# Kernel tuning notes

Hardware: AMD Instinct MI355X
Metric: run time of the kernel (lower is better)

Reference implementation:

```python
import jax, jax.numpy as jnp
import numpy as np

N, E, F_IN, H, C, Q = 4096, 131072, 512, 64, 16, 6
ALPHA = 1.0
NITER = 2  # torch.svd_lowrank default power iterations


def setup_inputs() -> dict:
    key = jax.random.key(0)
    ks = jax.random.split(key, 12)
    rn = lambda k, s, sc=0.05: jax.random.normal(k, s, dtype=jnp.float32) * sc
    return {
        'x': jax.random.normal(ks[0], (N, F_IN), dtype=jnp.float32),
        'edge_index': jax.random.randint(ks[1], (2, E), 0, N, dtype=jnp.int32),
        'gcn1_w': rn(ks[2], (F_IN, H)), 'gcn1_b': jnp.zeros((H,), jnp.float32),
        'gcn2_w': rn(ks[3], (H, C)), 'gcn2_b': jnp.zeros((C,), jnp.float32),
        'ptd1_w1': rn(ks[4], (F_IN, H)), 'ptd1_b1': jnp.zeros((H,), jnp.float32),
        'ptd1_w2': rn(ks[5], (H, 1)), 'ptd1_b2': jnp.zeros((1,), jnp.float32),
        'ptd2_w1': rn(ks[6], (H, 32)), 'ptd2_b1': jnp.zeros((32,), jnp.float32),
        'ptd2_w2': rn(ks[7], (32, 1)), 'ptd2_b2': jnp.zeros((1,), jnp.float32),
        'omega1': jax.random.normal(ks[8], (N, Q), dtype=jnp.float32),
        'omega2': jax.random.normal(ks[9], (N, Q), dtype=jnp.float32),
    }


def _mlp2(x, w1, b1, w2, b2):
    return jax.nn.relu(x @ w1 + b1) @ w2 + b2


def _edge_gate(x, src, dst, w1, b1, w2, b2):
    # agg = ptd(x_src - x_dst)**2 ; test branch: s = alpha*sigmoid(agg), clipped to [0,1]
    agg = _mlp2(x[src] - x[dst], w1, b1, w2, b2)
    agg = agg * agg
    s = ALPHA * jax.nn.sigmoid(agg)
    return jnp.clip(s.reshape(-1), 0.0, 1.0)


def _gcn_conv(x, src, dst, ew, w, b):
    # PyG GCNConv with edge_weight: add self-loops (weight 1), symmetric norm, aggregate src->dst
    h = x @ w
    si = jnp.arange(N)
    s_full = jnp.concatenate([src, si])
    d_full = jnp.concatenate([dst, si])
    ew_full = jnp.concatenate([ew, jnp.ones((N,), ew.dtype)])
    deg = jax.ops.segment_sum(ew_full, d_full, num_segments=N)
    dis = jnp.where(deg > 0, jax.lax.rsqrt(jnp.maximum(deg, 1e-12)), 0.0)
    norm = dis[s_full] * ew_full * dis[d_full]
    out = jax.ops.segment_sum(norm[:, None] * h[s_full], d_full, num_segments=N)
    return out + b


def _svd_lowrank_V(A, omega):
    # torch.svd_lowrank(A, q=6, niter=2): randomized range finder + small SVD; returns V [N, Q]
    Qb, _ = jnp.linalg.qr(A @ omega)
    for _ in range(NITER):
        Z, _ = jnp.linalg.qr(A.T @ Qb)
        Qb, _ = jnp.linalg.qr(A @ Z)
    B = Qb.T @ A  # [Q, N]
    _, _, Vh = jnp.linalg.svd(B, full_matrices=False)
    return Vh.T  # [N, Q]


def _nuc_loss(aa, V, deflate_matmul):
    loss = jnp.float32(0.0)
    for k in range(Q):  # fixed small Q=6, structurally sequential deflation
        vi = aa @ V[:, k:k + 1]  # [N,1]
        vi = vi / jnp.linalg.norm(vi)
        vmv = (vi.T @ (aa @ vi))[0, 0]
        vv = (vi.T @ vi)[0, 0]
        loss = loss + jnp.sqrt(jnp.abs(vmv / vv))
        if k > 1:
            outer = vi @ vi.T
            aa = aa - (aa @ outer if deflate_matmul else aa * outer)
    return loss


def reference(x, edge_index, gcn1_w, gcn1_b, gcn2_w, gcn2_b,
              ptd1_w1, ptd1_b1, ptd1_w2, ptd1_b2,
              ptd2_w1, ptd2_b1, ptd2_w2, ptd2_b2, omega1, omega2):
    src, dst = edge_index[0], edge_index[1]

    s_1 = _edge_gate(x, src, dst, ptd1_w1, ptd1_b1, ptd1_w2, ptd1_b2)  # [E]
    x1 = jax.nn.relu(_gcn_conv(x, src, dst, s_1, gcn1_w, gcn1_b))  # [N,H], dropout off (eval)

    s_2 = _edge_gate(x1, src, dst, ptd2_w1, ptd2_b1, ptd2_w2, ptd2_b2)  # [E]
    x_out = _gcn_conv(x1, src, dst, s_2, gcn2_w, gcn2_b)  # [N,C]

    # consistency loss: MSE of centered gates against zeros
    consist = jnp.mean((s_1 - jnp.mean(s_1)) ** 2) + jnp.mean((s_2 - jnp.mean(s_2)) ** 2)

    # dense adjacencies (duplicate edges sum, as in to_dense_adj)
    s1d = jnp.zeros((N, N), jnp.float32).at[src, dst].add(s_1) + 1e-6
    s2d = jnp.zeros((N, N), jnp.float32).at[src, dst].add(s_2) + 1e-6
    aa1 = s1d @ s1d.T
    aa2 = s2d @ s2d.T

    V1 = _svd_lowrank_V(s1d, omega1)
    V2 = _svd_lowrank_V(s2d, omega2)
    nuc = _nuc_loss(aa1, V1, deflate_matmul=False) + _nuc_loss(aa2, V2, deflate_matmul=True)

    top2 = jax.lax.top_k(x_out, 2)[0]
    calib = -top2[:, 0] + top2[:, 1]

    return (jax.nn.log_softmax(x_out, axis=1),
            jax.nn.softmax(x_out, axis=1),
            0.01 * consist + 0.01 * nuc,
            s_1, s_2, jnp.mean(calib))
```

## Files before the change

### kernel.cpp

```cpp
#include <hip/hip_runtime.h>
#include <cmath>

constexpr int N = 4096;
constexpr int EDG = 131072;
constexpr float GEPS = 1e-6f;

__device__ __forceinline__ float* blk_sums(float* vals, int cnt) {
  __shared__ float part[4][16];
  __shared__ float tot[16];
  const int lane = threadIdx.x & 63, wv = threadIdx.x >> 6;
  for (int c = 0; c < cnt; ++c) {
    float v = vals[c];
    for (int off = 32; off; off >>= 1) v += __shfl_down(v, off);
    if (lane == 0) part[wv][c] = v;
  }
  __syncthreads();
  if (threadIdx.x == 0)
    for (int c = 0; c < cnt; ++c)
      tot[c] = part[0][c] + part[1][c] + part[2][c] + part[3][c];
  __syncthreads();
  return tot;
}

__global__ void hist_edges(const int* __restrict__ ei, int* __restrict__ cnt) {
  int e = blockIdx.x * 256 + threadIdx.x;
  atomicAdd(&cnt[ei[e]], 1);
  atomicAdd(&cnt[N + ei[EDG + e]], 1);
}

__global__ __launch_bounds__(256) void scan2x(const int* __restrict__ cnt,
                                              int* __restrict__ rowptr,
                                              int* __restrict__ cur) {
  const int b = blockIdx.x;
  const int* c = cnt + b * N;
  int* rp = rowptr + b * (N + 1);
  int* cu = cur + b * N;
  __shared__ int part[256];
  const int t = threadIdx.x;
  int local[16], s = 0;
  const int base = t * 16;
  for (int i = 0; i < 16; ++i) { local[i] = s; s += c[base + i]; }
  part[t] = s;
  __syncthreads();
  if (t == 0) {
    int acc = 0;
    for (int i = 0; i < 256; ++i) { int v = part[i]; part[i] = acc; acc += v; }
  }
  __syncthreads();
  const int off = part[t];
  for (int i = 0; i < 16; ++i) { rp[base + i] = off + local[i]; cu[base + i] = off + local[i]; }
  if (t == 255) rp[N] = off + s;
}

__global__ void scatter_edges(const int* __restrict__ ei, int* __restrict__ cur,
                              int* __restrict__ col_s, int* __restrict__ perm_s,
                              int* __restrict__ col_d, int* __restrict__ perm_d) {
  int e = blockIdx.x * 256 + threadIdx.x;
  int s = ei[e], d = ei[EDG + e];
  int ps = atomicAdd(&cur[s], 1);
  col_s[ps] = d; perm_s[ps] = e;
  int pd = atomicAdd(&cur[N + d], 1);
  col_d[pd] = s; perm_d[pd] = e;
}

__global__ void gather_w2(const float* __restrict__ s, const int* __restrict__ perm_s,
                          const int* __restrict__ perm_d, float* __restrict__ ws_,
                          float* __restrict__ wd_) {
  int p = blockIdx.x * 256 + threadIdx.x;
  ws_[p] = s[perm_s[p]];
  wd_[p] = s[perm_d[p]];
}

template<int F, int DIS>
__global__ __launch_bounds__(256) void spmm(const int* __restrict__ rowptr,
                                            const int* __restrict__ col,
                                            const float* __restrict__ w,
                                            const float* __restrict__ X,
                                            const float* __restrict__ dis,
                                            float* __restrict__ OUT,
                                            float* __restrict__ SC, int cs_idx,
                                            float eps, int osum, int ossq) {
  constexpr int ES = 64 / F;
  const int lane = threadIdx.x & 63;
  const int wv = threadIdx.x >> 6;
  const int f = lane & (F - 1);
  const int es = lane / F;
  const int r = blockIdx.x * 4 + wv;
  const int e0 = rowptr[r], e1 = rowptr[r + 1];
  float acc = 0.f;
  for (int e = e0 + es; e < e1; e += ES) {
    int c = col[e];
    float wx = w[e];
    if (DIS) wx *= dis[c];
    acc += wx * X[(size_t)c * F + f];
  }
#pragma unroll
  for (int off = F; off < 64; off <<= 1) acc += __shfl_xor(acc, off);
  float o = acc + ((cs_idx >= 0) ? eps * SC[cs_idx + f] : 0.f);
  if (es == 0) OUT[(size_t)r * F + f] = o;
  if (osum >= 0 || ossq >= 0) {
    __shared__ float bs[8], bq[8];
    if (threadIdx.x < F) { bs[threadIdx.x] = 0.f; bq[threadIdx.x] = 0.f; }
    __syncthreads();
    if (es == 0) {
      if (osum >= 0) atomicAdd(&bs[f], o);
      if (ossq >= 0) atomicAdd(&bq[f], o * o);
    }
    __syncthreads();
    if (threadIdx.x < F) {
      if (osum >= 0) atomicAdd(&SC[osum + threadIdx.x], bs[threadIdx.x]);
      if (ossq >= 0) atomicAdd(&SC[ossq + threadIdx.x], bq[threadIdx.x]);
    }
  }
}

template<int FA, int FB>
__global__ __launch_bounds__(256) void spmm2(const int* __restrict__ rowptr,
                                             const int* __restrict__ col,
                                             const float* __restrict__ wA,
                                             const float* __restrict__ wB,
                                             const float* __restrict__ XA,
                                             const float* __restrict__ XB,
                                             float* __restrict__ OA,
                                             float* __restrict__ OB,
                                             float* __restrict__ SC,
                                             int csA, int csB, float eps,
                                             int osumA, int ossqA, int osumB, int ossqB) {
  const int lane = threadIdx.x & 63;
  const int wv = threadIdx.x >> 6;
  const int half = lane >> 5;
  const int la = lane & 31;
  const int F = half ? FB : FA;
  const int f = la & (F - 1);
  const int es = la / F;
  const int ES = 32 / F;
  const int r = blockIdx.x * 4 + wv;
  const int e0 = rowptr[r], e1 = rowptr[r + 1];
  const float* w = half ? wB : wA;
  const float* X = half ? XB : XA;
  float acc = 0.f;
  for (int e = e0 + es; e < e1; e += ES)
    acc += w[e] * X[(size_t)col[e] * F + f];
  for (int off = F; off < 32; off <<= 1) acc += __shfl_xor(acc, off);
  const int cs = half ? csB : csA;
  float o = acc + ((cs >= 0) ? eps * SC[cs + f] : 0.f);
  if (es == 0) {
    float* O = half ? OB : OA;
    O[(size_t)r * F + f] = o;
  }
  if (osumA >= 0 || ossqA >= 0 || osumB >= 0 || ossqB >= 0) {
    __shared__ float bs[2][8], bq[2][8];
    if (threadIdx.x < 16) { bs[threadIdx.x >> 3][threadIdx.x & 7] = 0.f;
                            bq[threadIdx.x >> 3][threadIdx.x & 7] = 0.f; }
    __syncthreads();
    const int osum = half ? osumB : osumA, ossq = half ? ossqB : ossqA;
    if (es == 0) {
      if (osum >= 0) atomicAdd(&bs[half][f], o);
      if (ossq >= 0) atomicAdd(&bq[half][f], o * o);
    }
    __syncthreads();
    if (threadIdx.x < 16) {
      int h = threadIdx.x >> 3, ff = threadIdx.x & 7;
      int os_ = h ? osumB : osumA, oq_ = h ? ossqB : ossqA;
      int Fh = h ? FB : FA;
      if (os_ >= 0 && ff < Fh) atomicAdd(&SC[os_ + ff], bs[h][ff]);
      if (oq_ >= 0 && ff < Fh) atomicAdd(&SC[oq_ + ff], bq[h][ff]);
    }
  }
}

__global__ __launch_bounds__(256) void gemm512(const float* __restrict__ A,
                                               const float* __restrict__ W1,
                                               const float* __restrict__ W2,
                                               float* __restrict__ O1,
                                               float* __restrict__ O2) {
  __shared__ float As[16][33];
  __shared__ float Ws[32][128];
  const int t = threadIdx.x;
  const int r = t >> 4;
  const int cg = t & 15;
  const int r0 = blockIdx.x * 16;
  float acc[8];
#pragma unroll
  for (int j = 0; j < 8; ++j) acc[j] = 0.f;
  for (int k0 = 0; k0 < 512; k0 += 32) {
    __syncthreads();
    {
      int idx = t;
#pragma unroll
      for (int i = 0; i < 2; ++i, idx += 256) {
        int rr = idx >> 5, kk = idx & 31;
        As[rr][kk] = A[(size_t)(r0 + rr) * 512 + k0 + kk];
      }
    }
    for (int idx = t; idx < 32 * 128; idx += 256) {
      int kk = idx >> 7, c = idx & 127;
      Ws[kk][c] = (c < 64) ? W1[(size_t)(k0 + kk) * 64 + c]
                           : W2[(size_t)(k0 + kk) * 64 + c - 64];
    }
    __syncthreads();
#pragma unroll 4
    for (int kk = 0; kk < 32; ++kk) {
      float a = As[r][kk];
      const float* wr = &Ws[kk][cg * 8];
#pragma unroll
      for (int j = 0; j < 8; ++j) acc[j] += a * wr[j];
    }
  }
  int n = r0 + r;
  if (cg < 8) {
#pragma unroll
    for (int j = 0; j < 8; ++j) O1[(size_t)n * 64 + cg * 8 + j] = acc[j];
  } else {
#pragma unroll
    for (int j = 0; j < 8; ++j) O2[(size_t)n * 64 + (cg - 8) * 8 + j] = acc[j];
  }
}

__global__ __launch_bounds__(256) void gemm64(const float* __restrict__ A,
                                              const float* __restrict__ W1,
                                              const float* __restrict__ W2,
                                              float* __restrict__ O1,
                                              float* __restrict__ O2) {
  __shared__ float As[32][65];
  __shared__ float Ws[64][48];
  const int t = threadIdx.x;
  const int r = t >> 3;
  const int cg = t & 7;
  const int r0 = blockIdx.x * 32;
  for (int idx = t; idx < 32 * 64; idx += 256)
    As[idx >> 6][idx & 63] = A[(size_t)(r0 + (idx >> 6)) * 64 + (idx & 63)];
  for (int idx = t; idx < 64 * 48; idx += 256) {
    int kk = idx / 48, c = idx % 48;
    Ws[kk][c] = (c < 32) ? W1[kk * 32 + c] : W2[kk * 16 + c - 32];
  }
  __syncthreads();
  float acc[6] = {0.f, 0.f, 0.f, 0.f, 0.f, 0.f};
  for (int k = 0; k < 64; ++k) {
    float a = As[r][k];
#pragma unroll
    for (int j = 0; j < 6; ++j) acc[j] += a * Ws[k][cg + 8 * j];
  }
  int n = r0 + r;
#pragma unroll
  for (int j = 0; j < 6; ++j) {
    int c = cg + 8 * j;
    if (c < 32) O1[(size_t)n * 32 + c] = acc[j];
    else O2[(size_t)n * 16 + c - 32] = acc[j];
  }
}

__global__ void edge_gate1(const float* __restrict__ xw, const int* __restrict__ ei,
                           const float* __restrict__ b1, const float* __restrict__ w2,
                           const float* __restrict__ b2, float* __restrict__ s_out,
                           float* __restrict__ deg, float* __restrict__ SCs) {
  const int lane = threadIdx.x & 63;
  const int wave = threadIdx.x >> 6;
  const float b1v = b1[lane];
  const float w2v = w2[lane];
  const float b2s = b2[0];
  float lsum = 0.f, lssq = 0.f;
  for (int it = 0; it < 16; ++it) {
    const int e = blockIdx.x * 64 + it * 4 + wave;
    const int s = ei[e];
    const int d = ei[EDG + e];
    float g = xw[(size_t)s * 64 + lane] - xw[(size_t)d * 64 + lane] + b1v;
    g = fmaxf(g, 0.f) * w2v;
#pragma unroll
    for (int off = 32; off; off >>= 1) g += __shfl_down(g, off);
    if (lane == 0) {
      float agg = g + b2s;
      agg *= agg;
      float sv = 1.f / (1.f + __expf(-agg));
      s_out[e] = sv;
      atomicAdd(&deg[d], sv);
      lsum += sv; lssq += sv * sv;
    }
  }
  __shared__ float red[8];
  if (lane == 0) { red[wave] = lsum; red[4 + wave] = lssq; }
  __syncthreads();
  if (threadIdx.x == 0) {
    atomicAdd(&SCs[0], red[0] + red[1] + red[2] + red[3]);
    atomicAdd(&SCs[1], red[4] + red[5] + red[6] + red[7]);
  }
}

__global__ void edge_gate2(const float* __restrict__ xw, const int* __restrict__ ei,
                           const float* __restrict__ b1, const float* __restrict__ w2,
                           const float* __restrict__ b2, float* __restrict__ s_out,
                           float* __restrict__ deg, float* __restrict__ SCs) {
  const int half = threadIdx.x & 31;
  const int wi = threadIdx.x >> 5;
  const float b1v = b1[half];
  const float w2v = w2[half];
  const float b2s = b2[0];
  float lsum = 0.f, lssq = 0.f;
  for (int it = 0; it < 16; ++it) {
    const int e = blockIdx.x * 128 + it * 8 + wi;
    const int s = ei[e];
    const int d = ei[EDG + e];
    float g = xw[(size_t)s * 32 + half] - xw[(size_t)d * 32 + half] + b1v;
    g = fmaxf(g, 0.f) * w2v;
#pragma unroll
    for (int off = 16; off; off >>= 1) g += __shfl_down(g, off, 32);
    if (half == 0) {
      float agg = g + b2s;
      agg *= agg;
      float sv = 1.f / (1.f + __expf(-agg));
      s_out[e] = sv;
      atomicAdd(&deg[d], sv);
      lsum += sv; lssq += sv * sv;
    }
  }
  __shared__ float red[16];
  if (half == 0) { red[wi] = lsum; red[8 + wi] = lssq; }
  __syncthreads();
  if (threadIdx.x == 0) {
    float a = 0.f, b = 0.f;
    for (int i = 0; i < 8; ++i) { a += red[i]; b += red[8 + i]; }
    atomicAdd(&SCs[0], a);
    atomicAdd(&SCs[1], b);
  }
}

__global__ void make_dis(const float* __restrict__ deg, float* __restrict__ dis) {
  int n = blockIdx.x * 256 + threadIdx.x;
  dis[n] = rsqrtf(deg[n] + 1.0f);
}

__global__ void conv_epi64(const float* __restrict__ P, const float* __restrict__ h,
                           const float* __restrict__ dis, const float* __restrict__ bias,
                           float* __restrict__ out) {
  int i = blockIdx.x * 256 + threadIdx.x;
  int n = i >> 6, f = i & 63;
  float d = dis[n];
  float v = d * (P[i] + d * h[i]) + bias[f];
  out[i] = fmaxf(v, 0.f);
}

__global__ void conv2_softmax(const float* __restrict__ P, const float* __restrict__ h,
                              const float* __restrict__ dis, const float* __restrict__ bias,
                              float* __restrict__ ls, float* __restrict__ sm,
                              float* __restrict__ SC) {
  const int t = threadIdx.x;
  const int r = blockIdx.x * 256 + t;
  const float d = dis[r];
  float v[16];
  float mx = -3.0e38f, mx2 = -3.0e38f;
#pragma unroll
  for (int c = 0; c < 16; ++c) {
    v[c] = d * (P[(size_t)r * 16 + c] + d * h[(size_t)r * 16 + c]) + bias[c];
    if (v[c] > mx) { mx2 = mx; mx = v[c]; }
    else if (v[c] > mx2) mx2 = v[c];
  }
  float se = 0.f;
#pragma unroll
  for (int c = 0; c < 16; ++c) se += expf(v[c] - mx);
  const float lse = mx + logf(se);
#pragma unroll
  for (int c = 0; c < 16; ++c) {
    float z = v[c] - lse;
    ls[(size_t)r * 16 + c] = z;
    sm[(size_t)r * 16 + c] = expf(z);
  }
  float calib = mx2 - mx;
  float* tot = blk_sums(&calib, 1);
  if (t == 0) atomicAdd(&SC[4], tot[0]);
}

__global__ void gram2(const float* __restrict__ YA, const float* __restrict__ YB,
                      double* __restrict__ GA, double* __restrict__ GB) {
  const int t = threadIdx.x;
  const int lane = t & 63, wv = t >> 6;
  const int n = blockIdx.x * 256 + t;
  float g[42];
  {
    float ya[6], yb[6];
#pragma unroll
    for (int j = 0; j < 6; ++j) { ya[j] = YA[(size_t)n * 8 + j]; yb[j] = YB[(size_t)n * 8 + j]; }
    int p = 0;
#pragma unroll
    for (int i = 0; i < 6; ++i)
#pragma unroll
      for (int j = i; j < 6; ++j) { g[p] = ya[i] * ya[j]; g[21 + p] = yb[i] * yb[j]; ++p; }
  }
#pragma unroll
  for (int p = 0; p < 42; ++p)
    for (int off = 32; off; off >>= 1) g[p] += __shfl_down(g[p], off);
  __shared__ float part[4][42];
  if (lane == 0)
    for (int p = 0; p < 42; ++p) part[wv][p] = g[p];
  __syncthreads();
  if (t < 42) {
    float s = part[0][t] + part[1][t] + part[2][t] + part[3][t];
    if (t < 21) atomicAdd(&GA[t], (double)s);
    else atomicAdd(&GB[t - 21], (double)s);
  }
}

__global__ void chol2(float* __restrict__ YA, const double* __restrict__ GA, int csA,
                      float* __restrict__ YB, const double* __restrict__ GB, int csB,
                      float* __restrict__ SC) {
  __shared__ float Rs[2][36];
  if (threadIdx.x < 2) {
    const double* G = threadIdx.x ? GB : GA;
    double Gf[6][6];
    int p = 0;
    for (int i = 0; i < 6; ++i)
      for (int j = i; j < 6; ++j) { Gf[i][j] = G[p]; Gf[j][i] = G[p]; ++p; }
    double Rm[6][6];
    for (int i = 0; i < 6; ++i) for (int j = 0; j < 6; ++j) Rm[i][j] = 0.0;
    for (int j = 0; j < 6; ++j) {
      double s = Gf[j][j];
      for (int k = 0; k < j; ++k) s -= Rm[k][j] * Rm[k][j];
      double dj = sqrt(fmax(s, 1e-30));
      Rm[j][j] = dj;
      for (int i = j + 1; i < 6; ++i) {
        double v = Gf[j][i];
        for (int k = 0; k < j; ++k) v -= Rm[k][j] * Rm[k][i];
        Rm[j][i] = v / dj;
      }
    }
    for (int i = 0; i < 6; ++i)
      for (int j = 0; j < 6; ++j) Rs[threadIdx.x][i * 6 + j] = (float)Rm[i][j];
  }
  __syncthreads();
  int n = blockIdx.x * 256 + threadIdx.x;
  float vals[12];
  {
    float y[6], q[6];
#pragma unroll
    for (int j = 0; j < 6; ++j) y[j] = YA[(size_t)n * 8 + j];
#pragma unroll
    for (int j = 0; j < 6; ++j) {
      float s = y[j];
#pragma unroll
      for (int i = 0; i < 6; ++i)
        if (i < j) s -= q[i] * Rs[0][i * 6 + j];
      q[j] = s / Rs[0][j * 6 + j];
    }
#pragma unroll
    for (int j = 0; j < 6; ++j) { YA[(size_t)n * 8 + j] = q[j]; vals[j] = q[j]; }
  }
  {
    float y[6], q[6];
#pragma unroll
    for (int j = 0; j < 6; ++j) y[j] = YB[(size_t)n * 8 + j];
#pragma unroll
    for (int j = 0; j < 6; ++j) {
      float s = y[j];
#pragma unroll
      for (int i = 0; i < 6; ++i)
        if (i < j) s -= q[i] * Rs[1][i * 6 + j];
      q[j] = s / Rs[1][j * 6 + j];
    }
#pragma unroll
    for (int j = 0; j < 6; ++j) { YB[(size_t)n * 8 + j] = q[j]; vals[6 + j] = q[j]; }
  }
  float* tot = blk_sums(vals, 12);
  if (threadIdx.x == 0)
    for (int j = 0; j < 6; ++j) {
      atomicAdd(&SC[csA + j], tot[j]);
      atomicAdd(&SC[csB + j], tot[6 + j]);
    }
}

__global__ __launch_bounds__(128) void jacobi2(const double* __restrict__ GA,
                                               const double* __restrict__ GB,
                                               float* __restrict__ SMFA,
                                               float* __restrict__ SMFB) {
  const int wv = threadIdx.x >> 6;
  const int lane = threadIdx.x & 63;
  const double* G = wv ? GB : GA;
  float* SMF = wv ? SMFB : SMFA;
  double a[6], v[6];
#pragma unroll
  for (int j = 0; j < 6; ++j) { a[j] = 0.0; v[j] = 0.0; }
  if (lane < 6) {
    const int r = lane;
    for (int j = 0; j < 6; ++j) {
      int i0 = r < j ? r : j, j0 = r < j ? j : r;
      a[j] = G[i0 * 6 - i0 * (i0 - 1) / 2 + (j0 - i0)];
    }
    v[r] = 1.0;
  }
  for (int sweep = 0; sweep < 10; ++sweep) {
#pragma unroll
    for (int p = 0; p < 5; ++p)
#pragma unroll
      for (int q = p + 1; q < 6; ++q) {
        double apq = __shfl(a[q], p, 64);
        double app = __shfl(a[p], p, 64);
        double aqq = __shfl(a[q], q, 64);
        double c = 1.0, s = 0.0;
        if (fabs(apq) > 1e-300) {
          double tau = (aqq - app) / (2.0 * apq);
          double tt = (tau >= 0.0) ? 1.0 / (tau + sqrt(1.0 + tau * tau))
                                   : 1.0 / (tau - sqrt(1.0 + tau * tau));
          c = 1.0 / sqrt(1.0 + tt * tt); s = tt * c;
        }
        double ap_ = a[p], aq_ = a[q];
        a[p] = c * ap_ - s * aq_;
        a[q] = s * ap_ + c * aq_;
#pragma unroll
        for (int i = 0; i < 6; ++i) {
          double rp = __shfl(a[i], p, 64);
          double rq = __shfl(a[i], q, 64);
          if (lane == p) a[i] = c * rp - s * rq;
          if (lane == q) a[i] = s * rp + c * rq;
        }
        double vp_ = v[p], vq_ = v[q];
        v[p] = c * vp_ - s * vq_;
        v[q] = s * vp_ + c * vq_;
      }
  }
  __shared__ double diag[2][6];
  __shared__ double Vs[2][6][6];
  if (lane < 6) {
    diag[wv][lane] = a[lane];
    for (int j = 0; j < 6; ++j) Vs[wv][lane][j] = v[j];
  }
  __syncthreads();
  if (lane == 0) {
    int idx[6] = {0, 1, 2, 3, 4, 5};
    for (int x = 0; x < 5; ++x)
      for (int b = 0; b < 5 - x; ++b)
        if (diag[wv][idx[b]] < diag[wv][idx[b + 1]]) {
          int tmp = idx[b]; idx[b] = idx[b + 1]; idx[b + 1] = tmp;
        }
    for (int k = 0; k < 6; ++k) {
      double lam = diag[wv][idx[k]];
      SMF[36 + k] = (float)(1.0 / sqrt(fmax(lam, 1e-30)));
      for (int j = 0; j < 6; ++j) SMF[j * 6 + k] = (float)Vs[wv][j][idx[k]];
    }
  }
}

__global__ void v_scale2(const float* __restrict__ BtA, const float* __restrict__ SMFA,
                         const float* __restrict__ BtB, const float* __restrict__ SMFB,
                         float* __restrict__ V8A, float* __restrict__ V8B) {
  __shared__ float WsA[36], rsA[6], WsB[36], rsB[6];
  if (threadIdx.x < 36) { WsA[threadIdx.x] = SMFA[threadIdx.x]; WsB[threadIdx.x] = SMFB[threadIdx.x]; }
  if (threadIdx.x < 6) { rsA[threadIdx.x] = SMFA[36 + threadIdx.x]; rsB[threadIdx.x] = SMFB[36 + threadIdx.x]; }
  __syncthreads();
  int n = blockIdx.x * 256 + threadIdx.x;
  float ba[6], bb[6];
#pragma unroll
  for (int j = 0; j < 6; ++j) { ba[j] = BtA[(size_t)n * 8 + j]; bb[j] = BtB[(size_t)n * 8 + j]; }
#pragma unroll
  for (int k = 0; k < 6; ++k) {
    float sa = 0.f, sb = 0.f;
#pragma unroll
    for (int j = 0; j < 6; ++j) { sa += ba[j] * WsA[j * 6 + k]; sb += bb[j] * WsB[j * 6 + k]; }
    V8A[(size_t)n * 8 + k] = sa * rsA[k];
    V8B[(size_t)n * 8 + k] = sb * rsB[k];
  }
  V8A[(size_t)n * 8 + 6] = 0.f; V8A[(size_t)n * 8 + 7] = 0.f;
  V8B[(size_t)n * 8 + 6] = 0.f; V8B[(size_t)n * 8 + 7] = 0.f;
}

__global__ void pad8c2(const float* __restrict__ o1, float* __restrict__ d1,
                       const float* __restrict__ o2, float* __restrict__ d2,
                       float* __restrict__ SC, int s1, int s2) {
  int n = blockIdx.x * 256 + threadIdx.x;
  float vals[12];
#pragma unroll
  for (int k = 0; k < 6; ++k) {
    vals[k] = o1[(size_t)n * 6 + k];     d1[(size_t)n * 8 + k] = vals[k];
    vals[6 + k] = o2[(size_t)n * 6 + k]; d2[(size_t)n * 8 + k] = vals[6 + k];
  }
  d1[(size_t)n * 8 + 6] = 0.f; d1[(size_t)n * 8 + 7] = 0.f;
  d2[(size_t)n * 8 + 6] = 0.f; d2[(size_t)n * 8 + 7] = 0.f;
  float* tot = blk_sums(vals, 12);
  if (threadIdx.x == 0)
    for (int c = 0; c < 6; ++c) {
      atomicAdd(&SC[s1 + c], tot[c]);
      atomicAdd(&SC[s2 + c], tot[6 + c]);
    }
}

__global__ void pack3c2(const float* __restrict__ V8A, float* __restrict__ WA,
                        const float* __restrict__ V8B, float* __restrict__ WB,
                        float* __restrict__ SC, int sA, int sB) {
  int n = blockIdx.x * 256 + threadIdx.x;
  float vals[6];
#pragma unroll
  for (int k = 0; k < 3; ++k) {
    vals[k] = V8A[(size_t)n * 8 + k];     WA[(size_t)n * 4 + k] = vals[k];
    vals[3 + k] = V8B[(size_t)n * 8 + k]; WB[(size_t)n * 4 + k] = vals[3 + k];
  }
  WA[(size_t)n * 4 + 3] = 0.f;
  WB[(size_t)n * 4 + 3] = 0.f;
  float* tot = blk_sums(vals, 6);
  if (threadIdx.x == 0)
    for (int c = 0; c < 3; ++c) {
      atomicAdd(&SC[sA + c], tot[c]);
      atomicAdd(&SC[sB + c], tot[3 + c]);
    }
}

__global__ void build_Wc(float* __restrict__ out, int FCpad, int nterms, int nu,
                         const float* __restrict__ base, int bstride, int boff,
                         const float* __restrict__ U, const float* __restrict__ SCin,
                         int rs_idx, float* __restrict__ SC, int sum_idx) {
  int n = blockIdx.x * 256 + threadIdx.x;
  float bv = base[(size_t)n * bstride + boff];
  if (rs_idx >= 0) bv *= rsqrtf(SCin[rs_idx]);
  float uv[3];
  for (int b = 0; b < 3; ++b) uv[b] = (b < nu) ? U[(size_t)b * N + n] : 0.f;
  float vals[8];
  for (int t = 0; t < FCpad; ++t) {
    float v = 0.f;
    if (t < nterms) {
      v = bv;
      for (int b = 0; b < nu; ++b)
        if ((t >> b) & 1) v *= uv[b];
    }
    out[(size_t)n * FCpad + t] = v;
    vals[t] = v;
  }
  float* tot = blk_sums(vals, nterms);
  if (threadIdx.x == 0)
    for (int c = 0; c < nterms; ++c) atomicAdd(&SC[sum_idx + c], tot[c]);
}

__global__ void buildAB(float* __restrict__ WA, int FCpad, int nt, int nu,
                        const float* __restrict__ V8A, int kcol,
                        const float* __restrict__ UvA, float* __restrict__ SC, int sWa,
                        float* __restrict__ WB, const float* __restrict__ V8B,
                        const float* __restrict__ UvB, int nd, int sWb, int Cidx) {
  const int bid = blockIdx.x;
  const int n = (bid & 15) * 256 + threadIdx.x;
  if (bid < 16) {
    float bv = V8A[(size_t)n * 8 + kcol];
    float uv[3];
    for (int b = 0; b < 3; ++b) uv[b] = (b < nu) ? UvA[(size_t)b * N + n] : 0.f;
    float vals[8];
    for (int t = 0; t < FCpad; ++t) {
      float v = 0.f;
      if (t < nt) {
        v = bv;
        for (int b = 0; b < nu; ++b)
          if ((t >> b) & 1) v *= uv[b];
      }
      WA[(size_t)n * FCpad + t] = v;
      vals[t] = v;
    }
    float* tot = blk_sums(vals, nt);
    if (threadIdx.x == 0)
      for (int c = 0; c < nt; ++c) atomicAdd(&SC[sWa + c], tot[c]);
  } else {
    float v = V8B[(size_t)n * 8 + kcol];
    WB[(size_t)n * 4 + 0] = v;
    WB[(size_t)n * 4 + 1] = 0.f;
    WB[(size_t)n * 4 + 2] = 0.f;
    WB[(size_t)n * 4 + 3] = 0.f;
    float vals[4];
    vals[0] = v;
    for (int t = 0; t < 3; ++t) vals[1 + t] = (t < nd) ? UvB[(size_t)t * N + n] * v : 0.f;
    float* tot = blk_sums(vals, 1 + nd);
    if (threadIdx.x == 0) {
      atomicAdd(&SC[sWb], tot[0]);
      for (int t = 0; t < nd; ++t) atomicAdd(&SC[Cidx + t], tot[1 + t]);
    }
  }
}

__global__ void epiAB(const float* __restrict__ YA, int FA, int nt, int nu,
                      const float* __restrict__ UvA, float* __restrict__ yvA, int nyA2,
                      const float* __restrict__ YB, const float* __restrict__ Pv,
                      const float* __restrict__ UvB, int nd, float* __restrict__ yvB,
                      int Cidx, int nyB2, int dp, float* __restrict__ SC) {
  const int bid = blockIdx.x;
  const int n = (bid & 15) * 256 + threadIdx.x;
  if (bid < 16) {
    float uv[3];
    for (int b = 0; b < 3; ++b) uv[b] = (b < nu) ? UvA[(size_t)b * N + n] : 0.f;
    float s = 0.f;
    for (int t = 0; t < nt; ++t) {
      float w = YA[(size_t)n * FA + t];
      int pc = 0;
      for (int b = 0; b < nu; ++b)
        if ((t >> b) & 1) { w *= uv[b]; ++pc; }
      s += (pc & 1) ? -w : w;
    }
    yvA[n] = s;
    float v = s * s;
    float* tot = blk_sums(&v, 1);
    if (threadIdx.x == 0) atomicAdd(&SC[nyA2], tot[0]);
  } else {
    float y = YB[(size_t)n * 4];
    for (int t = 0; t < nd; ++t) y -= SC[Cidx + t] * Pv[(size_t)t * N + n];
    yvB[n] = y;
    float vals[7];
    vals[0] = y * y;
    for (int t = 0; t < 3; ++t) {
      vals[1 + 2 * t] = (t < nd) ? y * Pv[(size_t)t * N + n] : 0.f;
      vals[2 + 2 * t] = (t < nd) ? UvB[(size_t)t * N + n] * y : 0.f;
    }
    float* tot = blk_sums(vals, 1 + 2 * nd);
    if (threadIdx.x == 0) {
      atomicAdd(&SC[nyB2], tot[0]);
      for (int i = 0; i < 2 * nd; ++i) atomicAdd(&SC[dp + i], tot[1 + i]);
    }
  }
}

__global__ void buildAB2(float* __restrict__ WA, int FCpad, int nt, int nu,
                         const float* __restrict__ yvA, const float* __restrict__ UvA,
                         int sW2a, float* __restrict__ WB,
                         const float* __restrict__ yvB, int sW2b,
                         float* __restrict__ SC) {
  const int bid = blockIdx.x;
  const int n = (bid & 15) * 256 + threadIdx.x;
  if (bid < 16) {
    float bv = yvA[n];
    float uv[3];
    for (int b = 0; b < 3; ++b) uv[b] = (b < nu) ? UvA[(size_t)b * N + n] : 0.f;
    float vals[8];
    for (int t = 0; t < FCpad; ++t) {
      float v = 0.f;
      if (t < nt) {
        v = bv;
        for (int b = 0; b < nu; ++b)
          if ((t >> b) & 1) v *= uv[b];
      }
      WA[(size_t)n * FCpad + t] = v;
      vals[t] = v;
    }
    float* tot = blk_sums(vals, nt);
    if (threadIdx.x == 0)
      for (int c = 0; c < nt; ++c) atomicAdd(&SC[sW2a + c], tot[c]);
  } else {
    float v = yvB[n];
    WB[(size_t)n * 4 + 0] = v;
    WB[(size_t)n * 4 + 1] = 0.f;
    WB[(size_t)n * 4 + 2] = 0.f;
    WB[(size_t)n * 4 + 3] = 0.f;
    float vv = v;
    float* tot = blk_sums(&vv, 1);
    if (threadIdx.x == 0) atomicAdd(&SC[sW2b], tot[0]);
  }
}

__global__ void vscale2(float* __restrict__ o1, const float* __restrict__ i1,
                        int s1, int f1, int r1,
                        float* __restrict__ o2, const float* __restrict__ i2,
                        int s2, int f2, int r2, const float* __restrict__ SC) {
  int n = blockIdx.x * 256 + threadIdx.x;
  float v1 = i1[(size_t)n * s1 + f1];
  if (r1 >= 0) v1 *= rsqrtf(SC[r1]);
  o1[n] = v1;
  float v2 = i2[(size_t)n * s2 + f2];
  if (r2 >= 0) v2 *= rsqrtf(SC[r2]);
  o2[n] = v2;
}

__global__ void vscale1(float* __restrict__ out, const float* __restrict__ in,
                        int stride, int off, const float* __restrict__ SC, int rs_idx) {
  int n = blockIdx.x * 256 + threadIdx.x;
  float v = in[(size_t)n * stride + off];
  if (rs_idx >= 0) v *= rsqrtf(SC[rs_idx]);
  out[n] = v;
}

__global__ void axpy_sq(float* __restrict__ out, const float* __restrict__ Y, int stride,
                        int off, const float* __restrict__ q0, const float* __restrict__ q1,
                        const float* __restrict__ q2, float* __restrict__ SC,
                        int c0, int c1, int c2, int np, int coef_rs, int out_rs,
                        int ssq_idx) {
  int n = blockIdx.x * 256 + threadIdx.x;
  float crs = (coef_rs >= 0) ? rsqrtf(SC[coef_rs]) : 1.f;
  float s = Y[(size_t)n * stride + off];
  if (np > 0) s -= SC[c0] * crs * q0[n];
  if (np > 1) s -= SC[c1] * crs * q1[n];
  if (np > 2) s -= SC[c2] * crs * q2[n];
  if (out_rs >= 0) s *= rsqrtf(SC[out_rs]);
  out[n] = s;
  if (ssq_idx >= 0) {
    float v = s * s;
    float* tot = blk_sums(&v, 1);
    if (threadIdx.x == 0) atomicAdd(&SC[ssq_idx], tot[0]);
  }
}

__global__ void accum2b(float* __restrict__ SC, int zA, int nyA, int zB, int nyB) {
  if (threadIdx.x || blockIdx.x) return;
  float add = 0.f;
  for (int k = 0; k < 3; ++k) add += sqrtf(fabsf(SC[zA + k] / SC[nyA + k]));
  for (int k = 0; k < 3; ++k) add += sqrtf(fabsf(SC[zB + k] / SC[nyB + k]));
  SC[5] += add;
}

__global__ void accum2k(float* __restrict__ SC, int zzA, int nt, int nyA,
                        int zzB, int nyB, int dp, int nd) {
  if (threadIdx.x || blockIdx.x) return;
  float vmv = 0.f;
  for (int t = 0; t < nt; ++t) {
    int pc = __popc(t);
    vmv += (pc & 1) ? -SC[zzA + t] : SC[zzA + t];
  }
  float add = sqrtf(fabsf(vmv / SC[nyA]));
  float vb = SC[zzB];
  for (int t = 0; t < nd; ++t) vb -= SC[dp + 2 * t] * SC[dp + 2 * t + 1];
  add += sqrtf(fabsf(vb / SC[nyB]));
  SC[5] += add;
}

__global__ void finalize_k(const float* __restrict__ SC, float* __restrict__ out) {
  if (threadIdx.x || blockIdx.x) return;
  const float Ef = (float)EDG;
  float m1 = SC[0] / Ef, v1 = SC[1] / Ef - m1 * m1;
  float m2 = SC[2] / Ef, v2 = SC[3] / Ef - m2 * m2;
  out[131072] = 0.01f * (v1 + v2) + 0.01f * SC[5];
  out[393217] = SC[4] / (float)N;
}

extern "C" void kernel_launch(void* const* d_in, const int* in_sizes, int n_in,
                              void* d_out, int out_size, void* d_ws, size_t ws_size,
                              hipStream_t stream) {
  const float* x      = (const float*)d_in[0];
  const int*   ei     = (const int*)  d_in[1];
  const float* gcn1_w = (const float*)d_in[2];
  const float* gcn1_b = (const float*)d_in[3];
  const float* gcn2_w = (const float*)d_in[4];
  const float* gcn2_b = (const float*)d_in[5];
  const float* p1w1   = (const float*)d_in[6];
  const float* p1b1   = (const float*)d_in[7];
  const float* p1w2   = (const float*)d_in[8];
  const float* p1b2   = (const float*)d_in[9];
  const float* p2w1   = (const float*)d_in[10];
  const float* p2b1   = (const float*)d_in[11];
  const float* p2w2   = (const float*)d_in[12];
  const float* p2b2   = (const float*)d_in[13];
  const float* omega1 = (const float*)d_in[14];
  const float* omega2 = (const float*)d_in[15];
  float* out = (float*)d_out;

  float* ws = (float*)d_ws;
  size_t o = 0;
  auto alloc = [&](size_t nf) { float* p = ws + o; o += nf; return p; };
  float* xw1  = alloc((size_t)N * 64);
  float* h1   = alloc((size_t)N * 64);
  float* x1   = alloc((size_t)N * 64);
  float* P    = alloc((size_t)N * 64);
  float* x1w  = alloc((size_t)N * 32);
  float* h2   = alloc((size_t)N * 16);
  float* P2   = alloc((size_t)N * 16);
  float* dis1 = alloc(N);
  float* dis2 = alloc(N);
  float* OmA  = alloc((size_t)N * 8);
  float* OmB  = alloc((size_t)N * 8);
  float* QA   = alloc((size_t)N * 8);
  float* QB   = alloc((size_t)N * 8);
  float* ZA   = alloc((size_t)N * 8);
  float* ZB   = alloc((size_t)N * 8);
  float* BtA  = alloc((size_t)N * 8);
  float* BtB  = alloc((size_t)N * 8);
  float* V8A  = alloc((size_t)N * 8);
  float* V8B  = alloc((size_t)N * 8);
  float* WA   = alloc((size_t)N * 8);
  float* WB   = alloc((size_t)N * 4);
  float* TA   = alloc((size_t)N * 8);
  float* TB   = alloc((size_t)N * 4);
  float* YA   = alloc((size_t)N * 8);
  float* YB   = alloc((size_t)N * 4);
  float* ZZA  = alloc((size_t)N * 8);
  float* ZZB  = alloc((size_t)N * 4);
  float* P4   = alloc((size_t)N * 4);
  float* yvA  = alloc(N);
  float* yvB  = alloc(N);
  float* UvA  = alloc((size_t)3 * N);
  float* UvB  = alloc((size_t)3 * N);
  float* Pv   = alloc((size_t)3 * N);
  float* SMFA = alloc(64);
  float* SMFB = alloc(64);
  int* rowptr = (int*)alloc(2 * (N + 1) + 2);
  int* cur    = (int*)alloc(2 * N);
  int* col_s  = (int*)alloc(EDG);
  int* perm_s = (int*)alloc(EDG);
  int* col_d  = (int*)alloc(EDG);
  int* perm_d = (int*)alloc(EDG);
  float* w1s  = alloc(EDG);
  float* w1d  = alloc(EDG);
  float* w2s  = alloc(EDG);
  float* w2d  = alloc(EDG);
  o = (o + 1) & ~(size_t)1;
  float* zb = ws + o;
  double* Gd = (double*)zb;            o += 288 * 2;
  int* cnt   = (int*)(ws + o);         o += 2 * N;
  float* deg1 = alloc(N);
  float* deg2 = alloc(N);
  float* SC   = alloc(1024);
  const size_t zero_bytes = (576 + 2 * N + 2 * N + 1024) * sizeof(float);
  if (ws_size < o * sizeof(float)) return;

  const int* rp_s = rowptr;
  const int* rp_d = rowptr + (N + 1);

  int cs = 8;
  auto NS = [&]() { int s = cs; cs += 8; return s; };
  int gslot = 0;
  auto NG = [&]() { int g = gslot; gslot += 24; return g; };

  hipMemsetAsync(zb, 0, zero_bytes, stream);
  hist_edges<<<512, 256, 0, stream>>>(ei, cnt);
  scan2x<<<2, 256, 0, stream>>>(cnt, rowptr, cur);
  scatter_edges<<<512, 256, 0, stream>>>(ei, cur, col_s, perm_s, col_d, perm_d);

  gemm512<<<256, 256, 0, stream>>>(x, p1w1, gcn1_w, xw1, h1);
  edge_gate1<<<2048, 256, 0, stream>>>(xw1, ei, p1b1, p1w2, p1b2,
                                       out + 131073, deg1, SC + 0);
  gather_w2<<<512, 256, 0, stream>>>(out + 131073, perm_s, perm_d, w1s, w1d);
  make_dis<<<16, 256, 0, stream>>>(deg1, dis1);
  spmm<64, 1><<<1024, 256, 0, stream>>>(rp_d, col_d, w1d, h1, dis1, P, SC, -1, 0.f, -1, -1);
  conv_epi64<<<1024, 256, 0, stream>>>(P, h1, dis1, gcn1_b, x1);

  gemm64<<<128, 256, 0, stream>>>(x1, p2w1, gcn2_w, x1w, h2);
  edge_gate2<<<1024, 256, 0, stream>>>(x1w, ei, p2b1, p2w2, p2b2,
                                       out + 262145, deg2, SC + 2);
  gather_w2<<<512, 256, 0, stream>>>(out + 262145, perm_s, perm_d, w2s, w2d);
  make_dis<<<16, 256, 0, stream>>>(deg2, dis2);
  spmm<16, 1><<<1024, 256, 0, stream>>>(rp_d, col_d, w2d, h2, dis2, P2, SC, -1, 0.f, -1, -1);
  conv2_softmax<<<16, 256, 0, stream>>>(P2, h2, dis2, gcn2_b, out, out + 65536, SC);

  {
    int s0a = NS(), s0b = NS();
    pad8c2<<<16, 256, 0, stream>>>(omega1, OmA, omega2, OmB, SC, s0a, s0b);
    spmm2<8, 8><<<1024, 256, 0, stream>>>(rp_s, col_s, w1s, w2s, OmA, OmB, QA, QB,
                                          SC, s0a, s0b, GEPS, -1, -1, -1, -1);
    int g0a = NG(), g0b = NG();
    gram2<<<16, 256, 0, stream>>>(QA, QB, Gd + g0a, Gd + g0b);
    int cqa = NS(), cqb = NS();
    chol2<<<16, 256, 0, stream>>>(QA, Gd + g0a, cqa, QB, Gd + g0b, cqb, SC);
    for (int itp = 0; itp < 2; ++itp) {
      spmm2<8, 8><<<1024, 256, 0, stream>>>(rp_d, col_d, w1d, w2d, QA, QB, ZA, ZB,
                                            SC, cqa, cqb, GEPS, -1, -1, -1, -1);
      int gza = NG(), gzb = NG();
      gram2<<<16, 256, 0, stream>>>(ZA, ZB, Gd + gza, Gd + gzb);
      int cza = NS(), czb = NS();
      chol2<<<16, 256, 0, stream>>>(ZA, Gd + gza, cza, ZB, Gd + gzb, czb, SC);
      spmm2<8, 8><<<1024, 256, 0, stream>>>(rp_s, col_s, w1s, w2s, ZA, ZB, QA, QB,
                                            SC, cza, czb, GEPS, -1, -1, -1, -1);
      int gqa = NG(), gqb = NG();
      gram2<<<16, 256, 0, stream>>>(QA, QB, Gd + gqa, Gd + gqb);
      cqa = NS(); cqb = NS();
      chol2<<<16, 256, 0, stream>>>(QA, Gd + gqa, cqa, QB, Gd + gqb, cqb, SC);
    }
    spmm2<8, 8><<<1024, 256, 0, stream>>>(rp_d, col_d, w1d, w2d, QA, QB, BtA, BtB,
                                          SC, cqa, cqb, GEPS, -1, -1, -1, -1);
    int gba = NG(), gbb = NG();
    gram2<<<16, 256, 0, stream>>>(BtA, BtB, Gd + gba, Gd + gbb);
    jacobi2<<<1, 128, 0, stream>>>(Gd + gba, Gd + gbb, SMFA, SMFB);
    v_scale2<<<16, 256, 0, stream>>>(BtA, SMFA, BtB, SMFB, V8A, V8B);
  }

  int nyB0;
  {
    int sWa = NS(), sWb = NS();
    pack3c2<<<16, 256, 0, stream>>>(V8A, WA, V8B, WB, SC, sWa, sWb);
    int sTa = NS(), sTb = NS();
    spmm2<4, 4><<<1024, 256, 0, stream>>>(rp_d, col_d, w1d, w2d, WA, WB, TA, TB,
                                          SC, sWa, sWb, GEPS, sTa, -1, sTb, -1);
    int sYa = NS(), sYb = NS(), nyA = NS(), nyB = NS();
    spmm2<4, 4><<<1024, 256, 0, stream>>>(rp_s, col_s, w1s, w2s, TA, TB, YA, YB,
                                          SC, sTa, sTb, GEPS, sYa, nyA, sYb, nyB);
    int zzA = NS(), zzB = NS();
    spmm2<4, 4><<<1024, 256, 0, stream>>>(rp_d, col_d, w1d, w2d, YA, YB, ZZA, ZZB,
                                          SC, sYa, sYb, GEPS, -1, zzA, -1, zzB);
    accum2b<<<1, 1, 0, stream>>>(SC, zzA, nyA, zzB, nyB);
    vscale2<<<16, 256, 0, stream>>>(UvA, YA, 4, 2, nyA + 2,
                                    UvB, YB, 4, 2, nyB + 2, SC);
    nyB0 = nyB;
  }

  {
    int sWp = NS();
    build_Wc<<<16, 256, 0, stream>>>(WB, 4, 1, 0, ZZB, 4, 2, nullptr, SC, nyB0 + 2, SC, sWp);
    spmm<4, 0><<<1024, 256, 0, stream>>>(rp_s, col_s, w2s, WB, nullptr, P4, SC, sWp, GEPS, -1, -1);
    vscale1<<<16, 256, 0, stream>>>(Pv, P4, 4, 0, SC, -1);
  }

  for (int k = 3; k <= 5; ++k) {
    const int nu = k - 2, nt = 1 << nu, nd = k - 2;
    const int FA = (k < 5) ? 4 : 8;
    int sWa = NS(), sWb = NS(), C = NS(), sTa = NS(), sTb = NS();
    int nyA2 = NS(), nyB2 = NS(), sW2a = NS(), sW2b = NS(), zzA2 = NS(), zzB2 = NS(), dp = NS();
    buildAB<<<32, 256, 0, stream>>>(WA, FA, nt, nu, V8A, k, UvA, SC, sWa,
                                    WB, V8B, UvB, nd, sWb, C);
    if (FA == 4) {
      spmm2<4, 4><<<1024, 256, 0, stream>>>(rp_d, col_d, w1d, w2d, WA, WB, TA, TB,
                                            SC, sWa, sWb, GEPS, sTa, -1, sTb, -1);
      spmm2<4, 4><<<1024, 256, 0, stream>>>(rp_s, col_s, w1s, w2s, TA, TB, YA, YB,
                                            SC, sTa, sTb, GEPS, -1, -1, -1, -1);
    } else {
      spmm2<8, 4><<<1024, 256, 0, stream>>>(rp_d, col_d, w1d, w2d, WA, WB, TA, TB,
                                            SC, sWa, sWb, GEPS, sTa, -1, sTb, -1);
      spmm2<8, 4><<<1024, 256, 0, stream>>>(rp_s, col_s, w1s, w2s, TA, TB, YA, YB,
                                            SC, sTa, sTb, GEPS, -1, -1, -1, -1);
    }
    epiAB<<<32, 256, 0, stream>>>(YA, FA, nt, nu, UvA, yvA, nyA2,
                                  YB, Pv, UvB, nd, yvB, C, nyB2, dp, SC);
    buildAB2<<<32, 256, 0, stream>>>(WA, FA, nt, nu, yvA, UvA, sW2a,
                                     WB, yvB, sW2b, SC);
    if (FA == 4)
      spmm2<4, 4><<<1024, 256, 0, stream>>>(rp_d, col_d, w1d, w2d, WA, WB, ZZA, ZZB,
                                            SC, sW2a, sW2b, GEPS, -1, zzA2, -1, zzB2);
    else
      spmm2<8, 4><<<1024, 256, 0, stream>>>(rp_d, col_d, w1d, w2d, WA, WB, ZZA, ZZB,
                                            SC, sW2a, sW2b, GEPS, -1, zzA2, -1, zzB2);
    accum2k<<<1, 1, 0, stream>>>(SC, zzA2, nt, nyA2, zzB2, nyB2, dp, nd);
    if (k < 5) {
      vscale2<<<16, 256, 0, stream>>>(UvA + (size_t)(k - 2) * N, yvA, 1, 0, nyA2,
                                      UvB + (size_t)(k - 2) * N, yvB, 1, 0, nyB2, SC);
      int sW3 = NS();
      build_Wc<<<16, 256, 0, stream>>>(WB, 4, 1, 0, ZZB, 4, 0, nullptr, SC, nyB2, SC, sW3);
      spmm<4, 0><<<1024, 256, 0, stream>>>(rp_s, col_s, w2s, WB, nullptr, P4, SC, sW3, GEPS, -1, -1);
      axpy_sq<<<16, 256, 0, stream>>>(Pv + (size_t)(k - 2) * N, P4, 4, 0,
                                      Pv, Pv + N, Pv + 2 * N,
                                      SC, dp + 1, dp + 3, dp + 5, nd, nyB2, -1, -1);
    }
  }

  finalize_k<<<1, 1, 0, stream>>>(SC, out);
}
```

Baseline: 863.4 us.

## Fuse SVD/nuclear-loss pipeline into one cooperative persistent kernel with grid syncs

Replaces dozens of small kernel launches for the randomized SVD and nuclear-norm stages with a single cooperative kernel of 256 blocks that steps through phases separated by grid-wide barriers. The goal is to remove per-launch overhead and idle gaps between many tiny dependent kernels. The GCN convolutions are also fused with their epilogues, make_dis is folded into the gather kernel, and the first GEMM is split along K with atomic accumulation. The cost is grid-sync latency, fewer resident blocks per phase, and reliance on cooperative launch residency.

```diff
diff --git a/kernel.cpp b/kernel.cpp
--- a/kernel.cpp
+++ b/kernel.cpp
@@ -1,26 +1,12 @@
 #include <hip/hip_runtime.h>
+#include <hip/hip_cooperative_groups.h>
 #include <cmath>
+
+namespace cg = cooperative_groups;
 
 constexpr int N = 4096;
 constexpr int EDG = 131072;
 constexpr float GEPS = 1e-6f;
-
-__device__ __forceinline__ float* blk_sums(float* vals, int cnt) {
-  __shared__ float part[4][16];
-  __shared__ float tot[16];
-  const int lane = threadIdx.x & 63, wv = threadIdx.x >> 6;
-  for (int c = 0; c < cnt; ++c) {
-    float v = vals[c];
-    for (int off = 32; off; off >>= 1) v += __shfl_down(v, off);
-    if (lane == 0) part[wv][c] = v;
-  }
-  __syncthreads();
-  if (threadIdx.x == 0)
-    for (int c = 0; c < cnt; ++c)
-      tot[c] = part[0][c] + part[1][c] + part[2][c] + part[3][c];
-  __syncthreads();
-  return tot;
-}
 
 __global__ void hist_edges(const int* __restrict__ ei, int* __restrict__ cnt) {
   int e = blockIdx.x * 256 + threadIdx.x;
@@ -63,157 +49,62 @@
   col_d[pd] = s; perm_d[pd] = e;
 }
 
-__global__ void gather_w2(const float* __restrict__ s, const int* __restrict__ perm_s,
+__global__ void gatherdis(const float* __restrict__ s, const int* __restrict__ perm_s,
                           const int* __restrict__ perm_d, float* __restrict__ ws_,
-                          float* __restrict__ wd_) {
+                          float* __restrict__ wd_, const float* __restrict__ deg,
+                          float* __restrict__ dis) {
   int p = blockIdx.x * 256 + threadIdx.x;
   ws_[p] = s[perm_s[p]];
   wd_[p] = s[perm_d[p]];
-}
-
-template<int F, int DIS>
-__global__ __launch_bounds__(256) void spmm(const int* __restrict__ rowptr,
-                                            const int* __restrict__ col,
-                                            const float* __restrict__ w,
-                                            const float* __restrict__ X,
-                                            const float* __restrict__ dis,
-                                            float* __restrict__ OUT,
-                                            float* __restrict__ SC, int cs_idx,
-                                            float eps, int osum, int ossq) {
-  constexpr int ES = 64 / F;
-  const int lane = threadIdx.x & 63;
-  const int wv = threadIdx.x >> 6;
-  const int f = lane & (F - 1);
-  const int es = lane / F;
-  const int r = blockIdx.x * 4 + wv;
-  const int e0 = rowptr[r], e1 = rowptr[r + 1];
-  float acc = 0.f;
-  for (int e = e0 + es; e < e1; e += ES) {
-    int c = col[e];
-    float wx = w[e];
-    if (DIS) wx *= dis[c];
-    acc += wx * X[(size_t)c * F + f];
-  }
-#pragma unroll
-  for (int off = F; off < 64; off <<= 1) acc += __shfl_xor(acc, off);
-  float o = acc + ((cs_idx >= 0) ? eps * SC[cs_idx + f] : 0.f);
-  if (es == 0) OUT[(size_t)r * F + f] = o;
-  if (osum >= 0 || ossq >= 0) {
-    __shared__ float bs[8], bq[8];
-    if (threadIdx.x < F) { bs[threadIdx.x] = 0.f; bq[threadIdx.x] = 0.f; }
-    __syncthreads();
-    if (es == 0) {
-      if (osum >= 0) atomicAdd(&bs[f], o);
-      if (ossq >= 0) atomicAdd(&bq[f], o * o);
-    }
-    __syncthreads();
-    if (threadIdx.x < F) {
-      if (osum >= 0) atomicAdd(&SC[osum + threadIdx.x], bs[threadIdx.x]);
-      if (ossq >= 0) atomicAdd(&SC[ossq + threadIdx.x], bq[threadIdx.x]);
-    }
-  }
-}
-
-template<int FA, int FB>
-__global__ __launch_bounds__(256) void spmm2(const int* __restrict__ rowptr,
-                                             const int* __restrict__ col,
-                                             const float* __restrict__ wA,
-                                             const float* __restrict__ wB,
-                                             const float* __restrict__ XA,
-                                             const float* __restrict__ XB,
-                                             float* __restrict__ OA,
-                                             float* __restrict__ OB,
-                                             float* __restrict__ SC,
-                                             int csA, int csB, float eps,
-                                             int osumA, int ossqA, int osumB, int ossqB) {
-  const int lane = threadIdx.x & 63;
-  const int wv = threadIdx.x >> 6;
-  const int half = lane >> 5;
-  const int la = lane & 31;
-  const int F = half ? FB : FA;
-  const int f = la & (F - 1);
-  const int es = la / F;
-  const int ES = 32 / F;
-  const int r = blockIdx.x * 4 + wv;
-  const int e0 = rowptr[r], e1 = rowptr[r + 1];
-  const float* w = half ? wB : wA;
-  const float* X = half ? XB : XA;
-  float acc = 0.f;
-  for (int e = e0 + es; e < e1; e += ES)
-    acc += w[e] * X[(size_t)col[e] * F + f];
-  for (int off = F; off < 32; off <<= 1) acc += __shfl_xor(acc, off);
-  const int cs = half ? csB : csA;
-  float o = acc + ((cs >= 0) ? eps * SC[cs + f] : 0.f);
-  if (es == 0) {
-    float* O = half ? OB : OA;
-    O[(size_t)r * F + f] = o;
-  }
-  if (osumA >= 0 || ossqA >= 0 || osumB >= 0 || ossqB >= 0) {
-    __shared__ float bs[2][8], bq[2][8];
-    if (threadIdx.x < 16) { bs[threadIdx.x >> 3][threadIdx.x & 7] = 0.f;
-                            bq[threadIdx.x >> 3][threadIdx.x & 7] = 0.f; }
-    __syncthreads();
-    const int osum = half ? osumB : osumA, ossq = half ? ossqB : ossqA;
-    if (es == 0) {
-      if (osum >= 0) atomicAdd(&bs[half][f], o);
-      if (ossq >= 0) atomicAdd(&bq[half][f], o * o);
-    }
-    __syncthreads();
-    if (threadIdx.x < 16) {
-      int h = threadIdx.x >> 3, ff = threadIdx.x & 7;
-      int os_ = h ? osumB : osumA, oq_ = h ? ossqB : ossqA;
-      int Fh = h ? FB : FA;
-      if (os_ >= 0 && ff < Fh) atomicAdd(&SC[os_ + ff], bs[h][ff]);
-      if (oq_ >= 0 && ff < Fh) atomicAdd(&SC[oq_ + ff], bq[h][ff]);
-    }
-  }
-}
-
-__global__ __launch_bounds__(256) void gemm512(const float* __restrict__ A,
-                                               const float* __restrict__ W1,
-                                               const float* __restrict__ W2,
-                                               float* __restrict__ O1,
-                                               float* __restrict__ O2) {
+  if (p < N) dis[p] = rsqrtf(deg[p] + 1.0f);
+}
+
+__global__ __launch_bounds__(256) void gemm512k(const float* __restrict__ A,
+                                                const float* __restrict__ W1,
+                                                const float* __restrict__ W2,
+                                                float* __restrict__ O1,
+                                                float* __restrict__ O2) {
   __shared__ float As[16][33];
   __shared__ float Ws[32][128];
   const int t = threadIdx.x;
-  const int r = t >> 4;
-  const int cg = t & 15;
+  const int rt = t >> 4;
+  const int ct = t & 15;
   const int r0 = blockIdx.x * 16;
+  const int kh = blockIdx.y * 256;
   float acc[8];
 #pragma unroll
   for (int j = 0; j < 8; ++j) acc[j] = 0.f;
-  for (int k0 = 0; k0 < 512; k0 += 32) {
+  for (int kc = 0; kc < 256; kc += 32) {
+    const int kb = kh + kc;
     __syncthreads();
-    {
-      int idx = t;
-#pragma unroll
-      for (int i = 0; i < 2; ++i, idx += 256) {
-        int rr = idx >> 5, kk = idx & 31;
-        As[rr][kk] = A[(size_t)(r0 + rr) * 512 + k0 + kk];
-      }
-    }
-    for (int idx = t; idx < 32 * 128; idx += 256) {
-      int kk = idx >> 7, c = idx & 127;
-      Ws[kk][c] = (c < 64) ? W1[(size_t)(k0 + kk) * 64 + c]
-                           : W2[(size_t)(k0 + kk) * 64 + c - 64];
+    for (int i = t; i < 512; i += 256) {
+      int rr = i >> 5, kk = i & 31;
+      As[rr][kk] = A[(size_t)(r0 + rr) * 512 + kb + kk];
+    }
+    for (int i = t; i < 1024; i += 256) {
+      int row = i >> 5, c4 = i & 31;
+      float4 v;
+      if (c4 < 16) v = *(const float4*)&W1[(size_t)(kb + row) * 64 + c4 * 4];
+      else         v = *(const float4*)&W2[(size_t)(kb + row) * 64 + (c4 - 16) * 4];
+      *(float4*)&Ws[row][c4 * 4] = v;
     }
     __syncthreads();
-#pragma unroll 4
+#pragma unroll
     for (int kk = 0; kk < 32; ++kk) {
-      float a = As[r][kk];
-      const float* wr = &Ws[kk][cg * 8];
-#pragma unroll
-      for (int j = 0; j < 8; ++j) acc[j] += a * wr[j];
-    }
-  }
-  int n = r0 + r;
-  if (cg < 8) {
-#pragma unroll
-    for (int j = 0; j < 8; ++j) O1[(size_t)n * 64 + cg * 8 + j] = acc[j];
-  } else {
-#pragma unroll
-    for (int j = 0; j < 8; ++j) O2[(size_t)n * 64 + (cg - 8) * 8 + j] = acc[j];
+      float a = As[rt][kk];
+      float4 b0 = *(const float4*)&Ws[kk][ct * 4];
+      float4 b1 = *(const float4*)&Ws[kk][64 + ct * 4];
+      acc[0] += a * b0.x; acc[1] += a * b0.y;
+      acc[2] += a * b0.z; acc[3] += a * b0.w;
+      acc[4] += a * b1.x; acc[5] += a * b1.y;
+      acc[6] += a * b1.z; acc[7] += a * b1.w;
+    }
+  }
+  const int r = r0 + rt;
+#pragma unroll
+  for (int j = 0; j < 4; ++j) {
+    atomicAdd(&O1[(size_t)r * 64 + ct * 4 + j], acc[j]);
+    atomicAdd(&O2[(size_t)r * 64 + ct * 4 + j], acc[4 + j]);
   }
 }
 
@@ -324,56 +215,148 @@
   }
 }
 
-__global__ void make_dis(const float* __restrict__ deg, float* __restrict__ dis) {
-  int n = blockIdx.x * 256 + threadIdx.x;
-  dis[n] = rsqrtf(deg[n] + 1.0f);
-}
-
-__global__ void conv_epi64(const float* __restrict__ P, const float* __restrict__ h,
-                           const float* __restrict__ dis, const float* __restrict__ bias,
-                           float* __restrict__ out) {
-  int i = blockIdx.x * 256 + threadIdx.x;
-  int n = i >> 6, f = i & 63;
-  float d = dis[n];
-  float v = d * (P[i] + d * h[i]) + bias[f];
-  out[i] = fmaxf(v, 0.f);
-}
-
-__global__ void conv2_softmax(const float* __restrict__ P, const float* __restrict__ h,
-                              const float* __restrict__ dis, const float* __restrict__ bias,
-                              float* __restrict__ ls, float* __restrict__ sm,
-                              float* __restrict__ SC) {
-  const int t = threadIdx.x;
-  const int r = blockIdx.x * 256 + t;
-  const float d = dis[r];
-  float v[16];
-  float mx = -3.0e38f, mx2 = -3.0e38f;
-#pragma unroll
-  for (int c = 0; c < 16; ++c) {
-    v[c] = d * (P[(size_t)r * 16 + c] + d * h[(size_t)r * 16 + c]) + bias[c];
-    if (v[c] > mx) { mx2 = mx; mx = v[c]; }
-    else if (v[c] > mx2) mx2 = v[c];
-  }
-  float se = 0.f;
-#pragma unroll
-  for (int c = 0; c < 16; ++c) se += expf(v[c] - mx);
-  const float lse = mx + logf(se);
-#pragma unroll
-  for (int c = 0; c < 16; ++c) {
-    float z = v[c] - lse;
-    ls[(size_t)r * 16 + c] = z;
-    sm[(size_t)r * 16 + c] = expf(z);
-  }
-  float calib = mx2 - mx;
-  float* tot = blk_sums(&calib, 1);
-  if (t == 0) atomicAdd(&SC[4], tot[0]);
-}
-
-__global__ void gram2(const float* __restrict__ YA, const float* __restrict__ YB,
-                      double* __restrict__ GA, double* __restrict__ GB) {
-  const int t = threadIdx.x;
-  const int lane = t & 63, wv = t >> 6;
-  const int n = blockIdx.x * 256 + t;
+__global__ void conv1f(const int* __restrict__ rp, const int* __restrict__ cl,
+                       const float* __restrict__ w, const float* __restrict__ h1,
+                       const float* __restrict__ dis, const float* __restrict__ bias,
+                       float* __restrict__ x1) {
+  const int lane = threadIdx.x & 63, wv = threadIdx.x >> 6;
+  const int r = blockIdx.x * 4 + wv;
+  const int e0 = rp[r], e1 = rp[r + 1];
+  float acc = 0.f;
+  for (int e = e0; e < e1; ++e) {
+    int c = cl[e];
+    acc += w[e] * dis[c] * h1[(size_t)c * 64 + lane];
+  }
+  float d = dis[r];
+  float v = d * (acc + d * h1[(size_t)r * 64 + lane]) + bias[lane];
+  x1[(size_t)r * 64 + lane] = fmaxf(v, 0.f);
+}
+
+__global__ void conv2f(const int* __restrict__ rp, const int* __restrict__ cl,
+                       const float* __restrict__ w, const float* __restrict__ h2,
+                       const float* __restrict__ dis, const float* __restrict__ bias,
+                       float* __restrict__ xo) {
+  const int lane = threadIdx.x & 63, wv = threadIdx.x >> 6;
+  const int f = lane & 15, es = lane >> 4;
+  const int r = blockIdx.x * 4 + wv;
+  const int e0 = rp[r], e1 = rp[r + 1];
+  float acc = 0.f;
+  for (int e = e0 + es; e < e1; e += 4) {
+    int c = cl[e];
+    acc += w[e] * dis[c] * h2[(size_t)c * 16 + f];
+  }
+  acc += __shfl_xor(acc, 16);
+  acc += __shfl_xor(acc, 32);
+  if (es == 0) {
+    float d = dis[r];
+    xo[(size_t)r * 16 + f] = d * (acc + d * h2[(size_t)r * 16 + f]) + bias[f];
+  }
+}
+
+struct KP {
+  const int *rp_s, *rp_d, *col_s, *col_d;
+  const float *w1s, *w1d, *w2s, *w2d;
+  const float *omega1, *omega2;
+  float *OmA, *OmB, *QA, *QB, *ZA, *ZB, *BtA, *BtB, *V8A, *V8B;
+  float *WA, *WB, *TA, *TB, *YA, *YB, *ZZA, *ZZB, *P4;
+  float *yvA, *yvB, *UvA, *UvB, *Pv, *SMFA, *SMFB;
+  const float *xo;
+  float *out, *SC;
+  double *Gd;
+};
+
+__device__ __forceinline__ float* blk_sums(float* shm, float* vals, int cnt) {
+  float* part = shm;
+  float* tot = shm + 64;
+  const int lane = threadIdx.x & 63, wv = threadIdx.x >> 6;
+  for (int c = 0; c < cnt; ++c) {
+    float v = vals[c];
+    for (int off = 32; off; off >>= 1) v += __shfl_down(v, off);
+    if (lane == 0) part[wv * 16 + c] = v;
+  }
+  __syncthreads();
+  if (threadIdx.x == 0)
+    for (int c = 0; c < cnt; ++c)
+      tot[c] = part[c] + part[16 + c] + part[32 + c] + part[48 + c];
+  __syncthreads();
+  return tot;
+}
+
+__device__ void d_spmm2(int gb, int logFA, int logFB,
+                        const int* __restrict__ rp, const int* __restrict__ cl,
+                        const float* __restrict__ wA, const float* __restrict__ wB,
+                        const float* __restrict__ XA, const float* __restrict__ XB,
+                        float* __restrict__ OA, float* __restrict__ OB,
+                        float* __restrict__ SC, int csA, int csB,
+                        int osumA, int ossqA, int osumB, int ossqB, float* shms) {
+  const int lane = threadIdx.x & 63;
+  const int wv = threadIdx.x >> 6;
+  const int half = lane >> 5;
+  const int la = lane & 31;
+  const int logF = half ? logFB : logFA;
+  const int F = 1 << logF;
+  const int f = la & (F - 1);
+  const int es = la >> logF;
+  const int ES = 32 >> logF;
+  const float* w = half ? wB : wA;
+  const float* X = half ? XB : XA;
+  float* O = half ? OB : OA;
+  const int csx = half ? csB : csA;
+  const int osum = half ? osumB : osumA;
+  const int ossq = half ? ossqB : ossqA;
+  const bool needsum = (osumA >= 0) || (ossqA >= 0) || (osumB >= 0) || (ossqB >= 0);
+  float* bs = shms;
+  float* bq = shms + 16;
+  if (needsum) {
+    if (threadIdx.x < 32) shms[threadIdx.x] = 0.f;
+    __syncthreads();
+  }
+  for (int rr = 0; rr < 4; ++rr) {
+    const int r = gb * 16 + wv * 4 + rr;
+    const int e0 = rp[r], e1 = rp[r + 1];
+    float acc = 0.f;
+    for (int e = e0 + es; e < e1; e += ES)
+      acc += w[e] * X[((size_t)cl[e] << logF) + f];
+    for (int off = F; off < 32; off <<= 1) acc += __shfl_xor(acc, off);
+    float o = acc + ((csx >= 0) ? GEPS * SC[csx + f] : 0.f);
+    if (es == 0) {
+      O[((size_t)r << logF) + f] = o;
+      if (osum >= 0) atomicAdd(&bs[half * 8 + f], o);
+      if (ossq >= 0) atomicAdd(&bq[half * 8 + f], o * o);
+    }
+  }
+  if (needsum) {
+    __syncthreads();
+    if (threadIdx.x < 16) {
+      int h = threadIdx.x >> 3, ff = threadIdx.x & 7;
+      int os_ = h ? osumB : osumA, oq_ = h ? ossqB : ossqA;
+      int Fh = h ? (1 << logFB) : (1 << logFA);
+      if (os_ >= 0 && ff < Fh) atomicAdd(&SC[os_ + ff], bs[h * 8 + ff]);
+      if (oq_ >= 0 && ff < Fh) atomicAdd(&SC[oq_ + ff], bq[h * 8 + ff]);
+    }
+  }
+}
+
+__device__ void d_spmm1(int gb, const int* __restrict__ rp, const int* __restrict__ cl,
+                        const float* __restrict__ w, const float* __restrict__ X,
+                        float* __restrict__ O, const float* __restrict__ SC, int csx) {
+  const int lane = threadIdx.x & 63, wv = threadIdx.x >> 6;
+  const int f = lane & 3, es = lane >> 2;
+  for (int rr = 0; rr < 4; ++rr) {
+    const int r = gb * 16 + wv * 4 + rr;
+    const int e0 = rp[r], e1 = rp[r + 1];
+    float acc = 0.f;
+    for (int e = e0 + es; e < e1; e += 16)
+      acc += w[e] * X[(size_t)cl[e] * 4 + f];
+    for (int off = 4; off < 64; off <<= 1) acc += __shfl_xor(acc, off);
+    if (es == 0) O[(size_t)r * 4 + f] = acc + GEPS * SC[csx + f];
+  }
+}
+
+__device__ void d_gram2(int gb, const float* __restrict__ YA, const float* __restrict__ YB,
+                        double* __restrict__ GA, double* __restrict__ GB, float* shmg) {
+  const int t = threadIdx.x, lane = t & 63, wv = t >> 6;
+  const int n = gb * 256 + t;
   float g[42];
   {
     float ya[6], yb[6];
@@ -388,21 +371,21 @@
 #pragma unroll
   for (int p = 0; p < 42; ++p)
     for (int off = 32; off; off >>= 1) g[p] += __shfl_down(g[p], off);
-  __shared__ float part[4][42];
   if (lane == 0)
-    for (int p = 0; p < 42; ++p) part[wv][p] = g[p];
+    for (int p = 0; p < 42; ++p) shmg[wv * 42 + p] = g[p];
   __syncthreads();
   if (t < 42) {
-    float s = part[0][t] + part[1][t] + part[2][t] + part[3][t];
+    float s = shmg[t] + shmg[42 + t] + shmg[84 + t] + shmg[126 + t];
     if (t < 21) atomicAdd(&GA[t], (double)s);
     else atomicAdd(&GB[t - 21], (double)s);
   }
-}
-
-__global__ void chol2(float* __restrict__ YA, const double* __restrict__ GA, int csA,
-                      float* __restrict__ YB, const double* __restrict__ GB, int csB,
-                      float* __restrict__ SC) {
-  __shared__ float Rs[2][36];
+  __syncthreads();
+}
+
+__device__ void d_chol2(int gb, float* __restrict__ YA, const double* __restrict__ GA, int csA,
+                        float* __restrict__ YB, const double* __restrict__ GB, int csB,
+                        float* __restrict__ SC, float* shmf, float* shmB) {
+  float* Rs = shmf;
   if (threadIdx.x < 2) {
     const double* G = threadIdx.x ? GB : GA;
     double Gf[6][6];
@@ -423,10 +406,10 @@
       }
     }
     for (int i = 0; i < 6; ++i)
-      for (int j = 0; j < 6; ++j) Rs[threadIdx.x][i * 6 + j] = (float)Rm[i][j];
-  }
-  __syncthreads();
-  int n = blockIdx.x * 256 + threadIdx.x;
+      for (int j = 0; j < 6; ++j) Rs[threadIdx.x * 36 + i * 6 + j] = (float)Rm[i][j];
+  }
+  __syncthreads();
+  const int n = gb * 256 + threadIdx.x;
   float vals[12];
   {
     float y[6], q[6];
@@ -437,8 +420,8 @@
       float s = y[j];
 #pragma unroll
       for (int i = 0; i < 6; ++i)
-        if (i < j) s -= q[i] * Rs[0][i * 6 + j];
-      q[j] = s / Rs[0][j * 6 + j];
+        if (i < j) s -= q[i] * Rs[i * 6 + j];
+      q[j] = s / Rs[j * 6 + j];
     }
 #pragma unroll
     for (int j = 0; j < 6; ++j) { YA[(size_t)n * 8 + j] = q[j]; vals[j] = q[j]; }
@@ -452,13 +435,13 @@
       float s = y[j];
 #pragma unroll
       for (int i = 0; i < 6; ++i)
-        if (i < j) s -= q[i] * Rs[1][i * 6 + j];
-      q[j] = s / Rs[1][j * 6 + j];
+        if (i < j) s -= q[i] * Rs[36 + i * 6 + j];
+      q[j] = s / Rs[36 + j * 6 + j];
     }
 #pragma unroll
     for (int j = 0; j < 6; ++j) { YB[(size_t)n * 8 + j] = q[j]; vals[6 + j] = q[j]; }
   }
-  float* tot = blk_sums(vals, 12);
+  float* tot = blk_sums(shmB, vals, 12);
   if (threadIdx.x == 0)
     for (int j = 0; j < 6; ++j) {
       atomicAdd(&SC[csA + j], tot[j]);
@@ -466,355 +449,431 @@
     }
 }
 
-__global__ __launch_bounds__(128) void jacobi2(const double* __restrict__ GA,
-                                               const double* __restrict__ GB,
-                                               float* __restrict__ SMFA,
-                                               float* __restrict__ SMFB) {
-  const int wv = threadIdx.x >> 6;
-  const int lane = threadIdx.x & 63;
-  const double* G = wv ? GB : GA;
-  float* SMF = wv ? SMFB : SMFA;
-  double a[6], v[6];
-#pragma unroll
-  for (int j = 0; j < 6; ++j) { a[j] = 0.0; v[j] = 0.0; }
-  if (lane < 6) {
-    const int r = lane;
-    for (int j = 0; j < 6; ++j) {
-      int i0 = r < j ? r : j, j0 = r < j ? j : r;
-      a[j] = G[i0 * 6 - i0 * (i0 - 1) / 2 + (j0 - i0)];
-    }
-    v[r] = 1.0;
-  }
-  for (int sweep = 0; sweep < 10; ++sweep) {
-#pragma unroll
-    for (int p = 0; p < 5; ++p)
-#pragma unroll
-      for (int q = p + 1; q < 6; ++q) {
-        double apq = __shfl(a[q], p, 64);
-        double app = __shfl(a[p], p, 64);
-        double aqq = __shfl(a[q], q, 64);
-        double c = 1.0, s = 0.0;
-        if (fabs(apq) > 1e-300) {
-          double tau = (aqq - app) / (2.0 * apq);
-          double tt = (tau >= 0.0) ? 1.0 / (tau + sqrt(1.0 + tau * tau))
-                                   : 1.0 / (tau - sqrt(1.0 + tau * tau));
-          c = 1.0 / sqrt(1.0 + tt * tt); s = tt * c;
+__device__ void d_jacobi2(const double* __restrict__ GA, const double* __restrict__ GB,
+                          float* __restrict__ SMFA, float* __restrict__ SMFB,
+                          double* shmd) {
+  const int t = threadIdx.x, wv = t >> 6, lane = t & 63;
+  double* diag = shmd;
+  double* Vs = shmd + 12;
+  if (wv < 2) {
+    const double* G = wv ? GB : GA;
+    double a[6], v[6];
+#pragma unroll
+    for (int j = 0; j < 6; ++j) { a[j] = 0.0; v[j] = 0.0; }
+    if (lane < 6) {
+      for (int j = 0; j < 6; ++j) {
+        int i0 = lane < j ? lane : j, j0 = lane < j ? j : lane;
+        a[j] = G[i0 * 6 - i0 * (i0 - 1) / 2 + (j0 - i0)];
+      }
+      v[lane] = 1.0;
+    }
+    for (int sweep = 0; sweep < 10; ++sweep) {
+#pragma unroll
+      for (int p = 0; p < 5; ++p)
+#pragma unroll
+        for (int q = p + 1; q < 6; ++q) {
+          double apq = __shfl(a[q], p, 64);
+          double app = __shfl(a[p], p, 64);
+          double aqq = __shfl(a[q], q, 64);
+          double c = 1.0, s = 0.0;
+          if (fabs(apq) > 1e-300) {
+            double tau = (aqq - app) / (2.0 * apq);
+            double tt = (tau >= 0.0) ? 1.0 / (tau + sqrt(1.0 + tau * tau))
+                                     : 1.0 / (tau - sqrt(1.0 + tau * tau));
+            c = 1.0 / sqrt(1.0 + tt * tt); s = tt * c;
+          }
+          double ap_ = a[p], aq_ = a[q];
+          a[p] = c * ap_ - s * aq_;
+          a[q] = s * ap_ + c * aq_;
+#pragma unroll
+          for (int i = 0; i < 6; ++i) {
+            double rp_ = __shfl(a[i], p, 64);
+            double rq_ = __shfl(a[i], q, 64);
+            if (lane == p) a[i] = c * rp_ - s * rq_;
+            if (lane == q) a[i] = s * rp_ + c * rq_;
+          }
+          double vp_ = v[p], vq_ = v[q];
+          v[p] = c * vp_ - s * vq_;
+          v[q] = s * vp_ + c * vq_;
         }
-        double ap_ = a[p], aq_ = a[q];
-        a[p] = c * ap_ - s * aq_;
-        a[q] = s * ap_ + c * aq_;
-#pragma unroll
-        for (int i = 0; i < 6; ++i) {
-          double rp = __shfl(a[i], p, 64);
-          double rq = __shfl(a[i], q, 64);
-          if (lane == p) a[i] = c * rp - s * rq;
-          if (lane == q) a[i] = s * rp + c * rq;
-        }
-        double vp_ = v[p], vq_ = v[q];
-        v[p] = c * vp_ - s * vq_;
-        v[q] = s * vp_ + c * vq_;
-      }
-  }
-  __shared__ double diag[2][6];
-  __shared__ double Vs[2][6][6];
-  if (lane < 6) {
-    diag[wv][lane] = a[lane];
-    for (int j = 0; j < 6; ++j) Vs[wv][lane][j] = v[j];
-  }
-  __syncthreads();
-  if (lane == 0) {
+    }
+    if (lane < 6) {
+      diag[wv * 6 + lane] = a[lane];
+      for (int j = 0; j < 6; ++j) Vs[wv * 36 + lane * 6 + j] = v[j];
+    }
+  }
+  __syncthreads();
+  if (t < 2) {
+    float* SMF = t ? SMFB : SMFA;
+    const int g = t;
     int idx[6] = {0, 1, 2, 3, 4, 5};
     for (int x = 0; x < 5; ++x)
       for (int b = 0; b < 5 - x; ++b)
-        if (diag[wv][idx[b]] < diag[wv][idx[b + 1]]) {
+        if (diag[g * 6 + idx[b]] < diag[g * 6 + idx[b + 1]]) {
           int tmp = idx[b]; idx[b] = idx[b + 1]; idx[b + 1] = tmp;
         }
     for (int k = 0; k < 6; ++k) {
-      double lam = diag[wv][idx[k]];
+      double lam = diag[g * 6 + idx[k]];
       SMF[36 + k] = (float)(1.0 / sqrt(fmax(lam, 1e-30)));
-      for (int j = 0; j < 6; ++j) SMF[j * 6 + k] = (float)Vs[wv][j][idx[k]];
-    }
-  }
-}
-
-__global__ void v_scale2(const float* __restrict__ BtA, const float* __restrict__ SMFA,
-                         const float* __restrict__ BtB, const float* __restrict__ SMFB,
-                         float* __restrict__ V8A, float* __restrict__ V8B) {
-  __shared__ float WsA[36], rsA[6], WsB[36], rsB[6];
-  if (threadIdx.x < 36) { WsA[threadIdx.x] = SMFA[threadIdx.x]; WsB[threadIdx.x] = SMFB[threadIdx.x]; }
-  if (threadIdx.x < 6) { rsA[threadIdx.x] = SMFA[36 + threadIdx.x]; rsB[threadIdx.x] = SMFB[36 + threadIdx.x]; }
-  __syncthreads();
-  int n = blockIdx.x * 256 + threadIdx.x;
-  float ba[6], bb[6];
-#pragma unroll
-  for (int j = 0; j < 6; ++j) { ba[j] = BtA[(size_t)n * 8 + j]; bb[j] = BtB[(size_t)n * 8 + j]; }
-#pragma unroll
-  for (int k = 0; k < 6; ++k) {
-    float sa = 0.f, sb = 0.f;
-#pragma unroll
-    for (int j = 0; j < 6; ++j) { sa += ba[j] * WsA[j * 6 + k]; sb += bb[j] * WsB[j * 6 + k]; }
-    V8A[(size_t)n * 8 + k] = sa * rsA[k];
-    V8B[(size_t)n * 8 + k] = sb * rsB[k];
-  }
-  V8A[(size_t)n * 8 + 6] = 0.f; V8A[(size_t)n * 8 + 7] = 0.f;
-  V8B[(size_t)n * 8 + 6] = 0.f; V8B[(size_t)n * 8 + 7] = 0.f;
-}
-
-__global__ void pad8c2(const float* __restrict__ o1, float* __restrict__ d1,
-                       const float* __restrict__ o2, float* __restrict__ d2,
-                       float* __restrict__ SC, int s1, int s2) {
-  int n = blockIdx.x * 256 + threadIdx.x;
-  float vals[12];
-#pragma unroll
-  for (int k = 0; k < 6; ++k) {
-    vals[k] = o1[(size_t)n * 6 + k];     d1[(size_t)n * 8 + k] = vals[k];
-    vals[6 + k] = o2[(size_t)n * 6 + k]; d2[(size_t)n * 8 + k] = vals[6 + k];
-  }
-  d1[(size_t)n * 8 + 6] = 0.f; d1[(size_t)n * 8 + 7] = 0.f;
-  d2[(size_t)n * 8 + 6] = 0.f; d2[(size_t)n * 8 + 7] = 0.f;
-  float* tot = blk_sums(vals, 12);
-  if (threadIdx.x == 0)
-    for (int c = 0; c < 6; ++c) {
-      atomicAdd(&SC[s1 + c], tot[c]);
-      atomicAdd(&SC[s2 + c], tot[6 + c]);
-    }
-}
-
-__global__ void pack3c2(const float* __restrict__ V8A, float* __restrict__ WA,
-                        const float* __restrict__ V8B, float* __restrict__ WB,
-                        float* __restrict__ SC, int sA, int sB) {
-  int n = blockIdx.x * 256 + threadIdx.x;
-  float vals[6];
-#pragma unroll
-  for (int k = 0; k < 3; ++k) {
-    vals[k] = V8A[(size_t)n * 8 + k];     WA[(size_t)n * 4 + k] = vals[k];
-    vals[3 + k] = V8B[(size_t)n * 8 + k]; WB[(size_t)n * 4 + k] = vals[3 + k];
-  }
-  WA[(size_t)n * 4 + 3] = 0.f;
-  WB[(size_t)n * 4 + 3] = 0.f;
-  float* tot = blk_sums(vals, 6);
-  if (threadIdx.x == 0)
-    for (int c = 0; c < 3; ++c) {
-      atomicAdd(&SC[sA + c], tot[c]);
-      atomicAdd(&SC[sB + c], tot[3 + c]);
-    }
-}
-
-__global__ void build_Wc(float* __restrict__ out, int FCpad, int nterms, int nu,
-                         const float* __restrict__ base, int bstride, int boff,
-                         const float* __restrict__ U, const float* __restrict__ SCin,
-                         int rs_idx, float* __restrict__ SC, int sum_idx) {
-  int n = blockIdx.x * 256 + threadIdx.x;
-  float bv = base[(size_t)n * bstride + boff];
-  if (rs_idx >= 0) bv *= rsqrtf(SCin[rs_idx]);
-  float uv[3];
-  for (int b = 0; b < 3; ++b) uv[b] = (b < nu) ? U[(size_t)b * N + n] : 0.f;
-  float vals[8];
-  for (int t = 0; t < FCpad; ++t) {
-    float v = 0.f;
-    if (t < nterms) {
-      v = bv;
-      for (int b = 0; b < nu; ++b)
-        if ((t >> b) & 1) v *= uv[b];
-    }
-    out[(size_t)n * FCpad + t] = v;
-    vals[t] = v;
-  }
-  float* tot = blk_sums(vals, nterms);
-  if (threadIdx.x == 0)
-    for (int c = 0; c < nterms; ++c) atomicAdd(&SC[sum_idx + c], tot[c]);
-}
-
-__global__ void buildAB(float* __restrict__ WA, int FCpad, int nt, int nu,
-                        const float* __restrict__ V8A, int kcol,
-                        const float* __restrict__ UvA, float* __restrict__ SC, int sWa,
-                        float* __restrict__ WB, const float* __restrict__ V8B,
-                        const float* __restrict__ UvB, int nd, int sWb, int Cidx) {
-  const int bid = blockIdx.x;
-  const int n = (bid & 15) * 256 + threadIdx.x;
-  if (bid < 16) {
-    float bv = V8A[(size_t)n * 8 + kcol];
-    float uv[3];
-    for (int b = 0; b < 3; ++b) uv[b] = (b < nu) ? UvA[(size_t)b * N + n] : 0.f;
-    float vals[8];
-    for (int t = 0; t < FCpad; ++t) {
-      float v = 0.f;
-      if (t < nt) {
-        v = bv;
-        for (int b = 0; b < nu; ++b)
-          if ((t >> b) & 1) v *= uv[b];
+      for (int j = 0; j < 6; ++j) SMF[j * 6 + k] = (float)Vs[g * 36 + j * 6 + idx[k]];
+    }
+  }
+  __syncthreads();
+}
+
+__global__ __launch_bounds__(256) void svdnuc(KP kp) {
+  cg::grid_group grid = cg::this_grid();
+  __shared__ float shmf[272];
+  __shared__ double shmd[96];
+  float* shmB = shmf + 96;
+  const int gb = blockIdx.x, t = threadIdx.x;
+  float* SC = kp.SC;
+
+  int cs = 8;
+  auto NS = [&]() { int s = cs; cs += 8; return s; };
+  int gslot = 0;
+  auto NG = [&]() { int g = gslot; gslot += 24; return g; };
+
+  int s0a = NS(), s0b = NS();
+  if (gb < 16) {
+    int n = gb * 256 + t;
+    float vals[12];
+#pragma unroll
+    for (int k = 0; k < 6; ++k) {
+      vals[k] = kp.omega1[(size_t)n * 6 + k];     kp.OmA[(size_t)n * 8 + k] = vals[k];
+      vals[6 + k] = kp.omega2[(size_t)n * 6 + k]; kp.OmB[(size_t)n * 8 + k] = vals[6 + k];
+    }
+    kp.OmA[(size_t)n * 8 + 6] = 0.f; kp.OmA[(size_t)n * 8 + 7] = 0.f;
+    kp.OmB[(size_t)n * 8 + 6] = 0.f; kp.OmB[(size_t)n * 8 + 7] = 0.f;
+    float* tot = blk_sums(shmB, vals, 12);
+    if (t == 0)
+      for (int c = 0; c < 6; ++c) {
+        atomicAdd(&SC[s0a + c], tot[c]);
+        atomicAdd(&SC[s0b + c], tot[6 + c]);
       }
-      WA[(size_t)n * FCpad + t] = v;
-      vals[t] = v;
-    }
-    float* tot = blk_sums(vals, nt);
-    if (threadIdx.x == 0)
-      for (int c = 0; c < nt; ++c) atomicAdd(&SC[sWa + c], tot[c]);
-  } else {
-    float v = V8B[(size_t)n * 8 + kcol];
-    WB[(size_t)n * 4 + 0] = v;
-    WB[(size_t)n * 4 + 1] = 0.f;
-    WB[(size_t)n * 4 + 2] = 0.f;
-    WB[(size_t)n * 4 + 3] = 0.f;
-    float vals[4];
-    vals[0] = v;
-    for (int t = 0; t < 3; ++t) vals[1 + t] = (t < nd) ? UvB[(size_t)t * N + n] * v : 0.f;
-    float* tot = blk_sums(vals, 1 + nd);
-    if (threadIdx.x == 0) {
-      atomicAdd(&SC[sWb], tot[0]);
-      for (int t = 0; t < nd; ++t) atomicAdd(&SC[Cidx + t], tot[1 + t]);
-    }
-  }
-}
-
-__global__ void epiAB(const float* __restrict__ YA, int FA, int nt, int nu,
-                      const float* __restrict__ UvA, float* __restrict__ yvA, int nyA2,
-                      const float* __restrict__ YB, const float* __restrict__ Pv,
-                      const float* __restrict__ UvB, int nd, float* __restrict__ yvB,
-                      int Cidx, int nyB2, int dp, float* __restrict__ SC) {
-  const int bid = blockIdx.x;
-  const int n = (bid & 15) * 256 + threadIdx.x;
-  if (bid < 16) {
-    float uv[3];
-    for (int b = 0; b < 3; ++b) uv[b] = (b < nu) ? UvA[(size_t)b * N + n] : 0.f;
-    float s = 0.f;
-    for (int t = 0; t < nt; ++t) {
-      float w = YA[(size_t)n * FA + t];
-      int pc = 0;
-      for (int b = 0; b < nu; ++b)
-        if ((t >> b) & 1) { w *= uv[b]; ++pc; }
-      s += (pc & 1) ? -w : w;
-    }
-    yvA[n] = s;
-    float v = s * s;
-    float* tot = blk_sums(&v, 1);
-    if (threadIdx.x == 0) atomicAdd(&SC[nyA2], tot[0]);
-  } else {
-    float y = YB[(size_t)n * 4];
-    for (int t = 0; t < nd; ++t) y -= SC[Cidx + t] * Pv[(size_t)t * N + n];
-    yvB[n] = y;
-    float vals[7];
-    vals[0] = y * y;
-    for (int t = 0; t < 3; ++t) {
-      vals[1 + 2 * t] = (t < nd) ? y * Pv[(size_t)t * N + n] : 0.f;
-      vals[2 + 2 * t] = (t < nd) ? UvB[(size_t)t * N + n] * y : 0.f;
-    }
-    float* tot = blk_sums(vals, 1 + 2 * nd);
-    if (threadIdx.x == 0) {
-      atomicAdd(&SC[nyB2], tot[0]);
-      for (int i = 0; i < 2 * nd; ++i) atomicAdd(&SC[dp + i], tot[1 + i]);
-    }
-  }
-}
-
-__global__ void buildAB2(float* __restrict__ WA, int FCpad, int nt, int nu,
-                         const float* __restrict__ yvA, const float* __restrict__ UvA,
-                         int sW2a, float* __restrict__ WB,
-                         const float* __restrict__ yvB, int sW2b,
-                         float* __restrict__ SC) {
-  const int bid = blockIdx.x;
-  const int n = (bid & 15) * 256 + threadIdx.x;
-  if (bid < 16) {
-    float bv = yvA[n];
-    float uv[3];
-    for (int b = 0; b < 3; ++b) uv[b] = (b < nu) ? UvA[(size_t)b * N + n] : 0.f;
-    float vals[8];
-    for (int t = 0; t < FCpad; ++t) {
-      float v = 0.f;
-      if (t < nt) {
-        v = bv;
-        for (int b = 0; b < nu; ++b)
-          if ((t >> b) & 1) v *= uv[b];
+  } else if (gb < 32) {
+    int r = (gb - 16) * 256 + t;
+    float v[16];
+    float mx = -3.0e38f, mx2 = -3.0e38f;
+#pragma unroll
+    for (int c = 0; c < 16; ++c) {
+      v[c] = kp.xo[(size_t)r * 16 + c];
+      if (v[c] > mx) { mx2 = mx; mx = v[c]; }
+      else if (v[c] > mx2) mx2 = v[c];
+    }
+    float se = 0.f;
+#pragma unroll
+    for (int c = 0; c < 16; ++c) se += expf(v[c] - mx);
+    const float lse = mx + logf(se);
+#pragma unroll
+    for (int c = 0; c < 16; ++c) {
+      float z = v[c] - lse;
+      kp.out[(size_t)r * 16 + c] = z;
+      kp.out[65536 + (size_t)r * 16 + c] = expf(z);
+    }
+    float calib = mx2 - mx;
+    float* tot = blk_sums(shmB, &calib, 1);
+    if (t == 0) atomicAdd(&SC[4], tot[0]);
+  }
+  grid.sync();
+
+  d_spmm2(gb, 3, 3, kp.rp_s, kp.col_s, kp.w1s, kp.w2s, kp.OmA, kp.OmB,
+          kp.QA, kp.QB, SC, s0a, s0b, -1, -1, -1, -1, shmf);
+  grid.sync();
+  int g0a = NG(), g0b = NG();
+  if (gb < 16) d_gram2(gb, kp.QA, kp.QB, kp.Gd + g0a, kp.Gd + g0b, shmB);
+  grid.sync();
+  int cqa = NS(), cqb = NS();
+  if (gb < 16) d_chol2(gb, kp.QA, kp.Gd + g0a, cqa, kp.QB, kp.Gd + g0b, cqb, SC, shmf, shmB);
+  grid.sync();
+  for (int itp = 0; itp < 2; ++itp) {
+    d_spmm2(gb, 3, 3, kp.rp_d, kp.col_d, kp.w1d, kp.w2d, kp.QA, kp.QB,
+            kp.ZA, kp.ZB, SC, cqa, cqb, -1, -1, -1, -1, shmf);
+    grid.sync();
+    int gza = NG(), gzb = NG();
+    if (gb < 16) d_gram2(gb, kp.ZA, kp.ZB, kp.Gd + gza, kp.Gd + gzb, shmB);
+    grid.sync();
+    int cza = NS(), czb = NS();
+    if (gb < 16) d_chol2(gb, kp.ZA, kp.Gd + gza, cza, kp.ZB, kp.Gd + gzb, czb, SC, shmf, shmB);
+    grid.sync();
+    d_spmm2(gb, 3, 3, kp.rp_s, kp.col_s, kp.w1s, kp.w2s, kp.ZA, kp.ZB,
+            kp.QA, kp.QB, SC, cza, czb, -1, -1, -1, -1, shmf);
+    grid.sync();
+    int gqa = NG(), gqb = NG();
+    if (gb < 16) d_gram2(gb, kp.QA, kp.QB, kp.Gd + gqa, kp.Gd + gqb, shmB);
+    grid.sync();
+    cqa = NS(); cqb = NS();
+    if (gb < 16) d_chol2(gb, kp.QA, kp.Gd + gqa, cqa, kp.QB, kp.Gd + gqb, cqb, SC, shmf, shmB);
+    grid.sync();
+  }
+  d_spmm2(gb, 3, 3, kp.rp_d, kp.col_d, kp.w1d, kp.w2d, kp.QA, kp.QB,
+          kp.BtA, kp.BtB, SC, cqa, cqb, -1, -1, -1, -1, shmf);
+  grid.sync();
+  int gba = NG(), gbb = NG();
+  if (gb < 16) d_gram2(gb, kp.BtA, kp.BtB, kp.Gd + gba, kp.Gd + gbb, shmB);
+  grid.sync();
+  if (gb == 0) d_jacobi2(kp.Gd + gba, kp.Gd + gbb, kp.SMFA, kp.SMFB, shmd);
+  grid.sync();
+  if (gb < 16) {
+    float* WsA = shmf;
+    float* rsA = shmf + 36;
+    float* WsB = shmf + 42;
+    float* rsB = shmf + 78;
+    if (t < 36) { WsA[t] = kp.SMFA[t]; WsB[t] = kp.SMFB[t]; }
+    if (t < 6) { rsA[t] = kp.SMFA[36 + t]; rsB[t] = kp.SMFB[36 + t]; }
+    __syncthreads();
+    int n = gb * 256 + t;
+    float ba[6], bb[6];
+#pragma unroll
+    for (int j = 0; j < 6; ++j) { ba[j] = kp.BtA[(size_t)n * 8 + j]; bb[j] = kp.BtB[(size_t)n * 8 + j]; }
+#pragma unroll
+    for (int k = 0; k < 6; ++k) {
+      float sa = 0.f, sb = 0.f;
+#pragma unroll
+      for (int j = 0; j < 6; ++j) { sa += ba[j] * WsA[j * 6 + k]; sb += bb[j] * WsB[j * 6 + k]; }
+      kp.V8A[(size_t)n * 8 + k] = sa * rsA[k];
+      kp.V8B[(size_t)n * 8 + k] = sb * rsB[k];
+    }
+    kp.V8A[(size_t)n * 8 + 6] = 0.f; kp.V8A[(size_t)n * 8 + 7] = 0.f;
+    kp.V8B[(size_t)n * 8 + 6] = 0.f; kp.V8B[(size_t)n * 8 + 7] = 0.f;
+  }
+  grid.sync();
+
+  int sWa = NS(), sWb = NS();
+  if (gb < 16) {
+    int n = gb * 256 + t;
+    float vals[6];
+#pragma unroll
+    for (int k = 0; k < 3; ++k) {
+      vals[k] = kp.V8A[(size_t)n * 8 + k];     kp.WA[(size_t)n * 4 + k] = vals[k];
+      vals[3 + k] = kp.V8B[(size_t)n * 8 + k]; kp.WB[(size_t)n * 4 + k] = vals[3 + k];
+    }
+    kp.WA[(size_t)n * 4 + 3] = 0.f;
+    kp.WB[(size_t)n * 4 + 3] = 0.f;
+    float* tot = blk_sums(shmB, vals, 6);
+    if (t == 0)
+      for (int c = 0; c < 3; ++c) {
+        atomicAdd(&SC[sWa + c], tot[c]);
+        atomicAdd(&SC[sWb + c], tot[3 + c]);
       }
-      WA[(size_t)n * FCpad + t] = v;
-      vals[t] = v;
-    }
-    float* tot = blk_sums(vals, nt);
-    if (threadIdx.x == 0)
-      for (int c = 0; c < nt; ++c) atomicAdd(&SC[sW2a + c], tot[c]);
-  } else {
-    float v = yvB[n];
-    WB[(size_t)n * 4 + 0] = v;
-    WB[(size_t)n * 4 + 1] = 0.f;
-    WB[(size_t)n * 4 + 2] = 0.f;
-    WB[(size_t)n * 4 + 3] = 0.f;
-    float vv = v;
-    float* tot = blk_sums(&vv, 1);
-    if (threadIdx.x == 0) atomicAdd(&SC[sW2b], tot[0]);
-  }
-}
-
-__global__ void vscale2(float* __restrict__ o1, const float* __restrict__ i1,
-                        int s1, int f1, int r1,
-                        float* __restrict__ o2, const float* __restrict__ i2,
-                        int s2, int f2, int r2, const float* __restrict__ SC) {
-  int n = blockIdx.x * 256 + threadIdx.x;
-  float v1 = i1[(size_t)n * s1 + f1];
-  if (r1 >= 0) v1 *= rsqrtf(SC[r1]);
-  o1[n] = v1;
-  float v2 = i2[(size_t)n * s2 + f2];
-  if (r2 >= 0) v2 *= rsqrtf(SC[r2]);
-  o2[n] = v2;
-}
-
-__global__ void vscale1(float* __restrict__ out, const float* __restrict__ in,
-                        int stride, int off, const float* __restrict__ SC, int rs_idx) {
-  int n = blockIdx.x * 256 + threadIdx.x;
-  float v = in[(size_t)n * stride + off];
-  if (rs_idx >= 0) v *= rsqrtf(SC[rs_idx]);
-  out[n] = v;
-}
-
-__global__ void axpy_sq(float* __restrict__ out, const float* __restrict__ Y, int stride,
-                        int off, const float* __restrict__ q0, const float* __restrict__ q1,
-                        const float* __restrict__ q2, float* __restrict__ SC,
-                        int c0, int c1, int c2, int np, int coef_rs, int out_rs,
-                        int ssq_idx) {
-  int n = blockIdx.x * 256 + threadIdx.x;
-  float crs = (coef_rs >= 0) ? rsqrtf(SC[coef_rs]) : 1.f;
-  float s = Y[(size_t)n * stride + off];
-  if (np > 0) s -= SC[c0] * crs * q0[n];
-  if (np > 1) s -= SC[c1] * crs * q1[n];
-  if (np > 2) s -= SC[c2] * crs * q2[n];
-  if (out_rs >= 0) s *= rsqrtf(SC[out_rs]);
-  out[n] = s;
-  if (ssq_idx >= 0) {
-    float v = s * s;
-    float* tot = blk_sums(&v, 1);
-    if (threadIdx.x == 0) atomicAdd(&SC[ssq_idx], tot[0]);
-  }
-}
-
-__global__ void accum2b(float* __restrict__ SC, int zA, int nyA, int zB, int nyB) {
-  if (threadIdx.x || blockIdx.x) return;
-  float add = 0.f;
-  for (int k = 0; k < 3; ++k) add += sqrtf(fabsf(SC[zA + k] / SC[nyA + k]));
-  for (int k = 0; k < 3; ++k) add += sqrtf(fabsf(SC[zB + k] / SC[nyB + k]));
-  SC[5] += add;
-}
-
-__global__ void accum2k(float* __restrict__ SC, int zzA, int nt, int nyA,
-                        int zzB, int nyB, int dp, int nd) {
-  if (threadIdx.x || blockIdx.x) return;
-  float vmv = 0.f;
-  for (int t = 0; t < nt; ++t) {
-    int pc = __popc(t);
-    vmv += (pc & 1) ? -SC[zzA + t] : SC[zzA + t];
-  }
-  float add = sqrtf(fabsf(vmv / SC[nyA]));
-  float vb = SC[zzB];
-  for (int t = 0; t < nd; ++t) vb -= SC[dp + 2 * t] * SC[dp + 2 * t + 1];
-  add += sqrtf(fabsf(vb / SC[nyB]));
-  SC[5] += add;
-}
-
-__global__ void finalize_k(const float* __restrict__ SC, float* __restrict__ out) {
-  if (threadIdx.x || blockIdx.x) return;
-  const float Ef = (float)EDG;
-  float m1 = SC[0] / Ef, v1 = SC[1] / Ef - m1 * m1;
-  float m2 = SC[2] / Ef, v2 = SC[3] / Ef - m2 * m2;
-  out[131072] = 0.01f * (v1 + v2) + 0.01f * SC[5];
-  out[393217] = SC[4] / (float)N;
+  }
+  grid.sync();
+  int sTa = NS(), sTb = NS();
+  d_spmm2(gb, 2, 2, kp.rp_d, kp.col_d, kp.w1d, kp.w2d, kp.WA, kp.WB,
+          kp.TA, kp.TB, SC, sWa, sWb, sTa, -1, sTb, -1, shmf);
+  grid.sync();
+  int sYa = NS(), sYb = NS(), nyA = NS(), nyB = NS();
+  d_spmm2(gb, 2, 2, kp.rp_s, kp.col_s, kp.w1s, kp.w2s, kp.TA, kp.TB,
+          kp.YA, kp.YB, SC, sTa, sTb, sYa, nyA, sYb, nyB, shmf);
+  grid.sync();
+  int zzA = NS(), zzB = NS();
+  d_spmm2(gb, 2, 2, kp.rp_d, kp.col_d, kp.w1d, kp.w2d, kp.YA, kp.YB,
+          kp.ZZA, kp.ZZB, SC, sYa, sYb, -1, zzA, -1, zzB, shmf);
+  grid.sync();
+  if (gb == 0 && t == 0) {
+    float add = 0.f;
+    for (int k = 0; k < 3; ++k) add += sqrtf(fabsf(SC[zzA + k] / SC[nyA + k]));
+    for (int k = 0; k < 3; ++k) add += sqrtf(fabsf(SC[zzB + k] / SC[nyB + k]));
+    SC[5] += add;
+  }
+  if (gb < 16) {
+    int n = gb * 256 + t;
+    kp.UvA[n] = kp.YA[(size_t)n * 4 + 2] * rsqrtf(SC[nyA + 2]);
+    kp.UvB[n] = kp.YB[(size_t)n * 4 + 2] * rsqrtf(SC[nyB + 2]);
+  }
+  grid.sync();
+  int sWp = NS();
+  if (gb < 16) {
+    int n = gb * 256 + t;
+    float v = kp.ZZB[(size_t)n * 4 + 2] * rsqrtf(SC[nyB + 2]);
+    kp.WB[(size_t)n * 4 + 0] = v;
+    kp.WB[(size_t)n * 4 + 1] = 0.f;
+    kp.WB[(size_t)n * 4 + 2] = 0.f;
+    kp.WB[(size_t)n * 4 + 3] = 0.f;
+    float* tot = blk_sums(shmB, &v, 1);
+    if (t == 0) atomicAdd(&SC[sWp], tot[0]);
+  }
+  grid.sync();
+  d_spmm1(gb, kp.rp_s, kp.col_s, kp.w2s, kp.WB, kp.P4, SC, sWp);
+  grid.sync();
+  if (gb < 16) {
+    int n = gb * 256 + t;
+    kp.Pv[n] = kp.P4[(size_t)n * 4 + 0];
+  }
+  grid.sync();
+
+  for (int k = 3; k <= 5; ++k) {
+    const int nu = k - 2, nt = 1 << nu, nd = k - 2;
+    const int logFA = (k < 5) ? 2 : 3;
+    const int FA = 1 << logFA;
+    int dWa = NS(), dWb = NS(), C = NS(), dTa = NS(), dTb = NS();
+    int nyA2 = NS(), nyB2 = NS(), sW2a = NS(), sW2b = NS(), zzA2 = NS(), zzB2 = NS(), dp = NS();
+    if (gb < 32) {
+      int n = (gb & 15) * 256 + t;
+      if (gb < 16) {
+        float bv = kp.V8A[(size_t)n * 8 + k];
+        float uv[3];
+        for (int b = 0; b < 3; ++b) uv[b] = (b < nu) ? kp.UvA[(size_t)b * N + n] : 0.f;
+        float vals[8];
+        for (int tt = 0; tt < FA; ++tt) {
+          float v = 0.f;
+          if (tt < nt) {
+            v = bv;
+            for (int b = 0; b < nu; ++b)
+              if ((tt >> b) & 1) v *= uv[b];
+          }
+          kp.WA[(size_t)n * FA + tt] = v;
+          vals[tt] = v;
+        }
+        float* tot = blk_sums(shmB, vals, nt);
+        if (t == 0)
+          for (int c = 0; c < nt; ++c) atomicAdd(&SC[dWa + c], tot[c]);
+      } else {
+        float v = kp.V8B[(size_t)n * 8 + k];
+        kp.WB[(size_t)n * 4 + 0] = v;
+        kp.WB[(size_t)n * 4 + 1] = 0.f;
+        kp.WB[(size_t)n * 4 + 2] = 0.f;
+        kp.WB[(size_t)n * 4 + 3] = 0.f;
+        float vals[4];
+        vals[0] = v;
+        for (int tt = 0; tt < 3; ++tt)
+          vals[1 + tt] = (tt < nd) ? kp.UvB[(size_t)tt * N + n] * v : 0.f;
+        float* tot = blk_sums(shmB, vals, 1 + nd);
+        if (t == 0) {
+          atomicAdd(&SC[dWb], tot[0]);
+          for (int tt = 0; tt < nd; ++tt) atomicAdd(&SC[C + tt], tot[1 + tt]);
+        }
+      }
+    }
+    grid.sync();
+    d_spmm2(gb, logFA, 2, kp.rp_d, kp.col_d, kp.w1d, kp.w2d, kp.WA, kp.WB,
+            kp.TA, kp.TB, SC, dWa, dWb, dTa, -1, dTb, -1, shmf);
+    grid.sync();
+    d_spmm2(gb, logFA, 2, kp.rp_s, kp.col_s, kp.w1s, kp.w2s, kp.TA, kp.TB,
+            kp.YA, kp.YB, SC, dTa, dTb, -1, -1, -1, -1, shmf);
+    grid.sync();
+    if (gb < 32) {
+      int n = (gb & 15) * 256 + t;
+      if (gb < 16) {
+        float uv[3];
+        for (int b = 0; b < 3; ++b) uv[b] = (b < nu) ? kp.UvA[(size_t)b * N + n] : 0.f;
+        float s = 0.f;
+        for (int tt = 0; tt < nt; ++tt) {
+          float w = kp.YA[(size_t)n * FA + tt];
+          int pc = 0;
+          for (int b = 0; b < nu; ++b)
+            if ((tt >> b) & 1) { w *= uv[b]; ++pc; }
+          s += (pc & 1) ? -w : w;
+        }
+        kp.yvA[n] = s;
+        float v = s * s;
+        float* tot = blk_sums(shmB, &v, 1);
+        if (t == 0) atomicAdd(&SC[nyA2], tot[0]);
+      } else {
+        float y = kp.YB[(size_t)n * 4];
+        for (int tt = 0; tt < nd; ++tt) y -= SC[C + tt] * kp.Pv[(size_t)tt * N + n];
+        kp.yvB[n] = y;
+        float vals[7];
+        vals[0] = y * y;
+        for (int tt = 0; tt < 3; ++tt) {
+          vals[1 + 2 * tt] = (tt < nd) ? y * kp.Pv[(size_t)tt * N + n] : 0.f;
+          vals[2 + 2 * tt] = (tt < nd) ? kp.UvB[(size_t)tt * N + n] * y : 0.f;
+        }
+        float* tot = blk_sums(shmB, vals, 1 + 2 * nd);
+        if (t == 0) {
+          atomicAdd(&SC[nyB2], tot[0]);
+          for (int i = 0; i < 2 * nd; ++i) atomicAdd(&SC[dp + i], tot[1 + i]);
+        }
+      }
+    }
+    grid.sync();
+    if (gb < 32) {
+      int n = (gb & 15) * 256 + t;
+      if (gb < 16) {
+        float bv = kp.yvA[n];
+        float uv[3];
+        for (int b = 0; b < 3; ++b) uv[b] = (b < nu) ? kp.UvA[(size_t)b * N + n] : 0.f;
+        float vals[8];
+        for (int tt = 0; tt < FA; ++tt) {
+          float v = 0.f;
+          if (tt < nt) {
+            v = bv;
+            for (int b = 0; b < nu; ++b)
+              if ((tt >> b) & 1) v *= uv[b];
+          }
+          kp.WA[(size_t)n * FA + tt] = v;
+          vals[tt] = v;
+        }
+        float* tot = blk_sums(shmB, vals, nt);
+        if (t == 0)
+          for (int c = 0; c < nt; ++c) atomicAdd(&SC[sW2a + c], tot[c]);
+      } else {
+        float v = kp.yvB[n];
+        kp.WB[(size_t)n * 4 + 0] = v;
+        kp.WB[(size_t)n * 4 + 1] = 0.f;
+        kp.WB[(size_t)n * 4 + 2] = 0.f;
+        kp.WB[(size_t)n * 4 + 3] = 0.f;
+        float* tot = blk_sums(shmB, &v, 1);
+        if (t == 0) atomicAdd(&SC[sW2b], tot[0]);
+      }
+    }
+    grid.sync();
+    d_spmm2(gb, logFA, 2, kp.rp_d, kp.col_d, kp.w1d, kp.w2d, kp.WA, kp.WB,
+            kp.ZZA, kp.ZZB, SC, sW2a, sW2b, -1, zzA2, -1, zzB2, shmf);
+    grid.sync();
+    if (gb == 0 && t == 0) {
+      float vmv = 0.f;
+      for (int tt = 0; tt < nt; ++tt) {
+        int pc = __popc(tt);
+        vmv += (pc & 1) ? -SC[zzA2 + tt] : SC[zzA2 + tt];
+      }
+      float add = sqrtf(fabsf(vmv / SC[nyA2]));
+      float vb = SC[zzB2];
+      for (int tt = 0; tt < nd; ++tt) vb -= SC[dp + 2 * tt] * SC[dp + 2 * tt + 1];
+      add += sqrtf(fabsf(vb / SC[nyB2]));
+      SC[5] += add;
+    }
+    if (k < 5 && gb < 16) {
+      int n = gb * 256 + t;
+      kp.UvA[(size_t)(k - 2) * N + n] = kp.yvA[n] * rsqrtf(SC[nyA2]);
+      kp.UvB[(size_t)(k - 2) * N + n] = kp.yvB[n] * rsqrtf(SC[nyB2]);
+    }
+    grid.sync();
+    if (k < 5) {
+      int sW3 = NS();
+      if (gb < 16) {
+        int n = gb * 256 + t;
+        float v = kp.ZZB[(size_t)n * 4 + 0] * rsqrtf(SC[nyB2]);
+        kp.WB[(size_t)n * 4 + 0] = v;
+        kp.WB[(size_t)n * 4 + 1] = 0.f;
+        kp.WB[(size_t)n * 4 + 2] = 0.f;
+        kp.WB[(size_t)n * 4 + 3] = 0.f;
+        float* tot = blk_sums(shmB, &v, 1);
+        if (t == 0) atomicAdd(&SC[sW3], tot[0]);
+      }
+      grid.sync();
+      d_spmm1(gb, kp.rp_s, kp.col_s, kp.w2s, kp.WB, kp.P4, SC, sW3);
+      grid.sync();
+      if (gb < 16) {
+        int n = gb * 256 + t;
+        float crs = rsqrtf(SC[nyB2]);
+        float s = kp.P4[(size_t)n * 4 + 0];
+        if (nd > 0) s -= SC[dp + 1] * crs * kp.Pv[n];
+        if (nd > 1) s -= SC[dp + 3] * crs * kp.Pv[N + n];
+        if (nd > 2) s -= SC[dp + 5] * crs * kp.Pv[2 * N + n];
+        kp.Pv[(size_t)(k - 2) * N + n] = s;
+      }
+      grid.sync();
+    }
+  }
+
+  if (gb == 0 && t == 0) {
+    const float Ef = (float)EDG;
+    float m1 = SC[0] / Ef, v1 = SC[1] / Ef - m1 * m1;
+    float m2 = SC[2] / Ef, v2 = SC[3] / Ef - m2 * m2;
+    kp.out[131072] = 0.01f * (v1 + v2) + 0.01f * SC[5];
+    kp.out[393217] = SC[4] / (float)N;
+  }
 }
 
 extern "C" void kernel_launch(void* const* d_in, const int* in_sizes, int n_in,
@@ -843,11 +902,16 @@
   auto alloc = [&](size_t nf) { float* p = ws + o; o += nf; return p; };
   float* xw1  = alloc((size_t)N * 64);
   float* h1   = alloc((size_t)N * 64);
+  double* Gd  = (double*)(ws + o); o += 576;
+  int* cnt    = (int*)(ws + o);    o += 2 * N;
+  float* deg1 = alloc(N);
+  float* deg2 = alloc(N);
+  float* SC   = alloc(1024);
+  const size_t zero_bytes = o * sizeof(float);
   float* x1   = alloc((size_t)N * 64);
-  float* P    = alloc((size_t)N * 64);
   float* x1w  = alloc((size_t)N * 32);
   float* h2   = alloc((size_t)N * 16);
-  float* P2   = alloc((size_t)N * 16);
+  float* xo   = alloc((size_t)N * 16);
   float* dis1 = alloc(N);
   float* dis2 = alloc(N);
   float* OmA  = alloc((size_t)N * 8);
@@ -886,142 +950,39 @@
   float* w1d  = alloc(EDG);
   float* w2s  = alloc(EDG);
   float* w2d  = alloc(EDG);
-  o = (o + 1) & ~(size_t)1;
-  float* zb = ws + o;
-  double* Gd = (double*)zb;            o += 288 * 2;
-  int* cnt   = (int*)(ws + o);         o += 2 * N;
-  float* deg1 = alloc(N);
-  float* deg2 = alloc(N);
-  float* SC   = alloc(1024);
-  const size_t zero_bytes = (576 + 2 * N + 2 * N + 1024) * sizeof(float);
   if (ws_size < o * sizeof(float)) return;
 
   const int* rp_s = rowptr;
   const int* rp_d = rowptr + (N + 1);
 
-  int cs = 8;
-  auto NS = [&]() { int s = cs; cs += 8; return s; };
-  int gslot = 0;
-  auto NG = [&]() { int g = gslot; gslot += 24; return g; };
-
-  hipMemsetAsync(zb, 0, zero_bytes, stream);
+  hipMemsetAsync(ws, 0, zero_bytes, stream);
   hist_edges<<<512, 256, 0, stream>>>(ei, cnt);
   scan2x<<<2, 256, 0, stream>>>(cnt, rowptr, cur);
   scatter_edges<<<512, 256, 0, stream>>>(ei, cur, col_s, perm_s, col_d, perm_d);
 
-  gemm512<<<256, 256, 0, stream>>>(x, p1w1, gcn1_w, xw1, h1);
+  gemm512k<<<dim3(256, 2), 256, 0, stream>>>(x, p1w1, gcn1_w, xw1, h1);
   edge_gate1<<<2048, 256, 0, stream>>>(xw1, ei, p1b1, p1w2, p1b2,
-                                       out + 131073, deg1, SC + 0);
-  gather_w2<<<512, 256, 0, stream>>>(out + 131073, perm_s, perm_d, w1s, w1d);
-  make_dis<<<16, 256, 0, stream>>>(deg1, dis1);
-  spmm<64, 1><<<1024, 256, 0, stream>>>(rp_d, col_d, w1d, h1, dis1, P, SC, -1, 0.f, -1, -1);
-  conv_epi64<<<1024, 256, 0, stream>>>(P, h1, dis1, gcn1_b, x1);
+                                       out + 131073, deg1, SC);
+  gatherdis<<<512, 256, 0, stream>>>(out + 131073, perm_s, perm_d, w1s, w1d, deg1, dis1);
+  conv1f<<<1024, 256, 0, stream>>>(rp_d, col_d, w1d, h1, dis1, gcn1_b, x1);
 
   gemm64<<<128, 256, 0, stream>>>(x1, p2w1, gcn2_w, x1w, h2);
   edge_gate2<<<1024, 256, 0, stream>>>(x1w, ei, p2b1, p2w2, p2b2,
                                        out + 262145, deg2, SC + 2);
-  gather_w2<<<512, 256, 0, stream>>>(out + 262145, perm_s, perm_d, w2s, w2d);
-  make_dis<<<16, 256, 0, stream>>>(deg2, dis2);
-  spmm<16, 1><<<1024, 256, 0, stream>>>(rp_d, col_d, w2d, h2, dis2, P2, SC, -1, 0.f, -1, -1);
-  conv2_softmax<<<16, 256, 0, stream>>>(P2, h2, dis2, gcn2_b, out, out + 65536, SC);
-
-  {
-    int s0a = NS(), s0b = NS();
-    pad8c2<<<16, 256, 0, stream>>>(omega1, OmA, omega2, OmB, SC, s0a, s0b);
-    spmm2<8, 8><<<1024, 256, 0, stream>>>(rp_s, col_s, w1s, w2s, OmA, OmB, QA, QB,
-                                          SC, s0a, s0b, GEPS, -1, -1, -1, -1);
-    int g0a = NG(), g0b = NG();
-    gram2<<<16, 256, 0, stream>>>(QA, QB, Gd + g0a, Gd + g0b);
-    int cqa = NS(), cqb = NS();
-    chol2<<<16, 256, 0, stream>>>(QA, Gd + g0a, cqa, QB, Gd + g0b, cqb, SC);
-    for (int itp = 0; itp < 2; ++itp) {
-      spmm2<8, 8><<<1024, 256, 0, stream>>>(rp_d, col_d, w1d, w2d, QA, QB, ZA, ZB,
-                                            SC, cqa, cqb, GEPS, -1, -1, -1, -1);
-      int gza = NG(), gzb = NG();
-      gram2<<<16, 256, 0, stream>>>(ZA, ZB, Gd + gza, Gd + gzb);
-      int cza = NS(), czb = NS();
-      chol2<<<16, 256, 0, stream>>>(ZA, Gd + gza, cza, ZB, Gd + gzb, czb, SC);
-      spmm2<8, 8><<<1024, 256, 0, stream>>>(rp_s, col_s, w1s, w2s, ZA, ZB, QA, QB,
-                                            SC, cza, czb, GEPS, -1, -1, -1, -1);
-      int gqa = NG(), gqb = NG();
-      gram2<<<16, 256, 0, stream>>>(QA, QB, Gd + gqa, Gd + gqb);
-      cqa = NS(); cqb = NS();
-      chol2<<<16, 256, 0, stream>>>(QA, Gd + gqa, cqa, QB, Gd + gqb, cqb, SC);
-    }
-    spmm2<8, 8><<<1024, 256, 0, stream>>>(rp_d, col_d, w1d, w2d, QA, QB, BtA, BtB,
-                                          SC, cqa, cqb, GEPS, -1, -1, -1, -1);
-    int gba = NG(), gbb = NG();
-    gram2<<<16, 256, 0, stream>>>(BtA, BtB, Gd + gba, Gd + gbb);
-    jacobi2<<<1, 128, 0, stream>>>(Gd + gba, Gd + gbb, SMFA, SMFB);
-    v_scale2<<<16, 256, 0, stream>>>(BtA, SMFA, BtB, SMFB, V8A, V8B);
-  }
-
-  int nyB0;
-  {
-    int sWa = NS(), sWb = NS();
-    pack3c2<<<16, 256, 0, stream>>>(V8A, WA, V8B, WB, SC, sWa, sWb);
-    int sTa = NS(), sTb = NS();
-    spmm2<4, 4><<<1024, 256, 0, stream>>>(rp_d, col_d, w1d, w2d, WA, WB, TA, TB,
-                                          SC, sWa, sWb, GEPS, sTa, -1, sTb, -1);
-    int sYa = NS(), sYb = NS(), nyA = NS(), nyB = NS();
-    spmm2<4, 4><<<1024, 256, 0, stream>>>(rp_s, col_s, w1s, w2s, TA, TB, YA, YB,
-                                          SC, sTa, sTb, GEPS, sYa, nyA, sYb, nyB);
-    int zzA = NS(), zzB = NS();
-    spmm2<4, 4><<<1024, 256, 0, stream>>>(rp_d, col_d, w1d, w2d, YA, YB, ZZA, ZZB,
-                                          SC, sYa, sYb, GEPS, -1, zzA, -1, zzB);
-    accum2b<<<1, 1, 0, stream>>>(SC, zzA, nyA, zzB, nyB);
-    vscale2<<<16, 256, 0, stream>>>(UvA, YA, 4, 2, nyA + 2,
-                                    UvB, YB, 4, 2, nyB + 2, SC);
-    nyB0 = nyB;
-  }
-
-  {
-    int sWp = NS();
-    build_Wc<<<16, 256, 0, stream>>>(WB, 4, 1, 0, ZZB, 4, 2, nullptr, SC, nyB0 + 2, SC, sWp);
-    spmm<4, 0><<<1024, 256, 0, stream>>>(rp_s, col_s, w2s, WB, nullptr, P4, SC, sWp, GEPS, -1, -1);
-    vscale1<<<16, 256, 0, stream>>>(Pv, P4, 4, 0, SC, -1);
-  }
-
-  for (int k = 3; k <= 5; ++k) {
-    const int nu = k - 2, nt = 1 << nu, nd = k - 2;
-    const int FA = (k < 5) ? 4 : 8;
-    int sWa = NS(), sWb = NS(), C = NS(), sTa = NS(), sTb = NS();
-    int nyA2 = NS(), nyB2 = NS(), sW2a = NS(), sW2b = NS(), zzA2 = NS(), zzB2 = NS(), dp = NS();
-    buildAB<<<32, 256, 0, stream>>>(WA, FA, nt, nu, V8A, k, UvA, SC, sWa,
-                                    WB, V8B, UvB, nd, sWb, C);
-    if (FA == 4) {
-      spmm2<4, 4><<<1024, 256, 0, stream>>>(rp_d, col_d, w1d, w2d, WA, WB, TA, TB,
-                                            SC, sWa, sWb, GEPS, sTa, -1, sTb, -1);
-      spmm2<4, 4><<<1024, 256, 0, stream>>>(rp_s, col_s, w1s, w2s, TA, TB, YA, YB,
-                                            SC, sTa, sTb, GEPS, -1, -1, -1, -1);
-    } else {
-      spmm2<8, 4><<<1024, 256, 0, stream>>>(rp_d, col_d, w1d, w2d, WA, WB, TA, TB,
-                                            SC, sWa, sWb, GEPS, sTa, -1, sTb, -1);
-      spmm2<8, 4><<<1024, 256, 0, stream>>>(rp_s, col_s, w1s, w2s, TA, TB, YA, YB,
-                                            SC, sTa, sTb, GEPS, -1, -1, -1, -1);
-    }
-    epiAB<<<32, 256, 0, stream>>>(YA, FA, nt, nu, UvA, yvA, nyA2,
-                                  YB, Pv, UvB, nd, yvB, C, nyB2, dp, SC);
-    buildAB2<<<32, 256, 0, stream>>>(WA, FA, nt, nu, yvA, UvA, sW2a,
-                                     WB, yvB, sW2b, SC);
-    if (FA == 4)
-      spmm2<4, 4><<<1024, 256, 0, stream>>>(rp_d, col_d, w1d, w2d, WA, WB, ZZA, ZZB,
-                                            SC, sW2a, sW2b, GEPS, -1, zzA2, -1, zzB2);
-    else
-      spmm2<8, 4><<<1024, 256, 0, stream>>>(rp_d, col_d, w1d, w2d, WA, WB, ZZA, ZZB,
-                                            SC, sW2a, sW2b, GEPS, -1, zzA2, -1, zzB2);
-    accum2k<<<1, 1, 0, stream>>>(SC, zzA2, nt, nyA2, zzB2, nyB2, dp, nd);
-    if (k < 5) {
-      vscale2<<<16, 256, 0, stream>>>(UvA + (size_t)(k - 2) * N, yvA, 1, 0, nyA2,
-                                      UvB + (size_t)(k - 2) * N, yvB, 1, 0, nyB2, SC);
-      int sW3 = NS();
-      build_Wc<<<16, 256, 0, stream>>>(WB, 4, 1, 0, ZZB, 4, 0, nullptr, SC, nyB2, SC, sW3);
-      spmm<4, 0><<<1024, 256, 0, stream>>>(rp_s, col_s, w2s, WB, nullptr, P4, SC, sW3, GEPS, -1, -1);
-      axpy_sq<<<16, 256, 0, stream>>>(Pv + (size_t)(k - 2) * N, P4, 4, 0,
-                                      Pv, Pv + N, Pv + 2 * N,
-                                      SC, dp + 1, dp + 3, dp + 5, nd, nyB2, -1, -1);
-    }
-  }
-
-  finalize_k<<<1, 1, 0, stream>>>(SC, out);
-}
+  gatherdis<<<512, 256, 0, stream>>>(out + 262145, perm_s, perm_d, w2s, w2d, deg2, dis2);
+  conv2f<<<1024, 256, 0, stream>>>(rp_d, col_d, w2d, h2, dis2, gcn2_b, xo);
+
+  KP kp;
+  kp.rp_s = rp_s; kp.rp_d = rp_d; kp.col_s = col_s; kp.col_d = col_d;
+  kp.w1s = w1s; kp.w1d = w1d; kp.w2s = w2s; kp.w2d = w2d;
+  kp.omega1 = omega1; kp.omega2 = omega2;
+  kp.OmA = OmA; kp.OmB = OmB; kp.QA = QA; kp.QB = QB; kp.ZA = ZA; kp.ZB = ZB;
+  kp.BtA = BtA; kp.BtB = BtB; kp.V8A = V8A; kp.V8B = V8B;
+  kp.WA = WA; kp.WB = WB; kp.TA = TA; kp.TB = TB; kp.YA = YA; kp.YB = YB;
+  kp.ZZA = ZZA; kp.ZZB = ZZB; kp.P4 = P4;
+  kp.yvA = yvA; kp.yvB = yvB; kp.UvA = UvA; kp.UvB = UvB; kp.Pv = Pv;
+  kp.SMFA = SMFA; kp.SMFB = SMFB;
+  kp.xo = xo; kp.out = out; kp.SC = SC; kp.Gd = Gd;
+  void* kargs[] = {&kp};
+  hipLaunchCooperativeKernel((void*)svdnuc, dim3(256), dim3(256), kargs, 0, stream);
+}
```

Result: slower. 2.260 ms (+161.7%).
